# Kernel tuning notes

Hardware: AMD Instinct MI355X
Metric: run time of the kernel (lower is better)

## Reference

```python
import jax, jax.numpy as jnp
from jax import lax
import numpy as np

B, N, G, K = 4, 1024, 128, 32
D_MODEL, DEPTH, CLS = 384, 12, 40
D_INNER, D_STATE, D_CONV, DT_RANK = 768, 16, 4, 24
EPS = 1e-5
BN_SCALE = 1.0 / float(np.sqrt(1.0 + EPS))  # eval BN, running_mean=0, running_var=1


def layernorm(x, w, b):
    mu = x.mean(-1, keepdims=True)
    var = ((x - mu) ** 2).mean(-1, keepdims=True)
    return (x - mu) * lax.rsqrt(var + EPS) * w + b


def bn_eval(x, g, b):
    return x * (g * BN_SCALE) + b


def fps(xyz, n):
    Bb, Nn, _ = xyz.shape
    first = jnp.zeros((Bb,), jnp.int32)

    def step(carry, _):
        dmin, last = carry
        p = jnp.take_along_axis(xyz, last[:, None, None], axis=1)  # B,1,3
        dmin = jnp.minimum(dmin, jnp.sum((xyz - p) ** 2, -1))
        nxt = jnp.argmax(dmin, -1).astype(jnp.int32)
        return (dmin, nxt), nxt

    _, rest = lax.scan(step, (jnp.full((Bb, Nn), 1e10, xyz.dtype), first), None, length=n - 1)
    return jnp.concatenate([first[None, :], rest], 0).T  # B,G


def group_points(xyz):
    idx = fps(xyz, G)
    center = jnp.take_along_axis(xyz, idx[:, :, None], axis=1)            # B,G,3
    d2 = jnp.sum((center[:, :, None, :] - xyz[:, None, :, :]) ** 2, -1)   # B,G,N
    _, knn = lax.top_k(-d2, K)                                            # B,G,K
    nb = jax.vmap(lambda p, i: p[i])(xyz, knn)                            # B,G,K,3
    return nb - center[:, :, None, :], center


def encoder(pg, w1, b1, g1, bb1, w2, b2, w3, b3, g2, bb2, w4, b4):
    Bb, Gg, Kk, _ = pg.shape
    f = pg.reshape(Bb * Gg, Kk, 3)
    f = jax.nn.relu(bn_eval(f @ w1.T + b1, g1, bb1))                      # BG,K,128
    f = f @ w2.T + b2                                                     # BG,K,256
    fg = f.max(1, keepdims=True)
    f = jnp.concatenate([jnp.broadcast_to(fg, f.shape), f], -1)           # BG,K,512
    f = jax.nn.relu(bn_eval(f @ w3.T + b3, g2, bb2))
    f = f @ w4.T + b4
    return f.max(1).reshape(Bb, Gg, -1)                                   # B,G,C


def mamba_mixer(x, ipw, cw, cb, xpw, dpw, dpb, A_log, Dp, opw):
    L = x.shape[1]
    xz = x @ ipw.T                                                        # B,L,2*Di
    u, z = jnp.split(xz, 2, -1)
    up = jnp.pad(u, ((0, 0), (D_CONV - 1, 0), (0, 0)))                    # causal depthwise conv
    u = sum(up[:, k:k + L, :] * cw[:, k] for k in range(D_CONV)) + cb
    u = jax.nn.silu(u)
    xdb = u @ xpw.T
    dt, Bm, Cm = jnp.split(xdb, [DT_RANK, DT_RANK + D_STATE], -1)
    dt = jax.nn.softplus(dt @ dpw.T + dpb)                                # B,L,Di
    A = -jnp.exp(A_log)                                                   # Di,Ds

    def step(h, inp):
        dt_t, B_t, C_t, u_t = inp
        h = jnp.exp(dt_t[:, :, None] * A) * h + (dt_t * u_t)[:, :, None] * B_t[:, None, :]
        return h, jnp.einsum('bds,bs->bd', h, C_t)

    h0 = jnp.zeros((x.shape[0], D_INNER, D_STATE), x.dtype)
    _, ys = lax.scan(step, h0, (dt.swapaxes(0, 1), Bm.swapaxes(0, 1), Cm.swapaxes(0, 1), u.swapaxes(0, 1)))
    y = ys.swapaxes(0, 1) + u * Dp
    return (y * jax.nn.silu(z)) @ opw.T


def forward(pts, enc_w1, enc_b1, enc_bn1_g, enc_bn1_b, enc_w2, enc_b2, enc_w3, enc_b3,
            enc_bn2_g, enc_bn2_b, enc_w4, enc_b4, pos_w1, pos_b1, pos_w2, pos_b2,
            ln_w, ln_b, in_proj_w, conv_w, conv_b, x_proj_w, dt_proj_w, dt_proj_b,
            A_log, D_param, out_proj_w, normf_w, normf_b, norm_w, norm_b,
            head_w1, head_b1, head_bn1_g, head_bn1_b, head_w2, head_b2,
            head_bn2_g, head_bn2_b, head_w3, head_b3):
    nb, center = group_points(pts)
    tok = encoder(nb, enc_w1, enc_b1, enc_bn1_g, enc_bn1_b, enc_w2, enc_b2,
                  enc_w3, enc_b3, enc_bn2_g, enc_bn2_b, enc_w4, enc_b4)    # B,G,384
    pos = jax.nn.gelu(center @ pos_w1.T + pos_b1, approximate=False) @ pos_w2.T + pos_b2

    # PointMamba token reordering: sort by center x, y, z and concatenate -> L = 3G
    toks, poss = [], []
    for ax in range(3):
        o = jnp.argsort(center[:, :, ax], axis=-1)[:, :, None]
        toks.append(jnp.take_along_axis(tok, o, axis=1))
        poss.append(jnp.take_along_axis(pos, o, axis=1))
    tok = jnp.concatenate(toks, 1)
    pos = jnp.concatenate(poss, 1)

    h = tok + pos
    res = jnp.zeros_like(h)

    def layer_step(carry, p):
        h, res = carry
        lnw, lnb, ipw, cw, cb, xpw, dpw, dpb, Al, Dp, opw = p
        res = h + res
        x = layernorm(res, lnw, lnb)
        h = mamba_mixer(x, ipw, cw, cb, xpw, dpw, dpb, Al, Dp, opw)
        return (h, res), None

    (h, res), _ = lax.scan(layer_step, (h, res),
                           (ln_w, ln_b, in_proj_w, conv_w, conv_b, x_proj_w,
                            dt_proj_w, dt_proj_b, A_log, D_param, out_proj_w))
    x = layernorm(h + res, normf_w, normf_b)   # MixerModel.norm_f
    x = layernorm(x, norm_w, norm_b)           # PointMamba.norm
    feat = x.mean(1)                           # B,384
    h1 = jax.nn.relu(bn_eval(feat @ head_w1.T + head_b1, head_bn1_g, head_bn1_b))
    h2 = jax.nn.relu(bn_eval(h1 @ head_w2.T + head_b2, head_bn2_g, head_bn2_b))
    return h2 @ head_w3.T + head_b3            # B,CLS


def setup_inputs():
    key = jax.random.key(0)
    ks = iter(jax.random.split(key, 64))

    def rn(shape, s=0.02):
        return jax.random.normal(next(ks), shape, jnp.float32) * s

    inp = dict(
        pts=jax.random.normal(next(ks), (B, N, 3), jnp.float32),
        enc_w1=rn((128, 3), 0.1), enc_b1=jnp.zeros((128,)),
        enc_bn1_g=jnp.ones((128,)), enc_bn1_b=jnp.zeros((128,)),
        enc_w2=rn((256, 128), 0.05), enc_b2=jnp.zeros((256,)),
        enc_w3=rn((512, 512), 0.05), enc_b3=jnp.zeros((512,)),
        enc_bn2_g=jnp.ones((512,)), enc_bn2_b=jnp.zeros((512,)),
        enc_w4=rn((D_MODEL, 512), 0.05), enc_b4=jnp.zeros((D_MODEL,)),
        pos_w1=rn((128, 3), 0.1), pos_b1=jnp.zeros((128,)),
        pos_w2=rn((D_MODEL, 128), 0.05), pos_b2=jnp.zeros((D_MODEL,)),
        ln_w=jnp.ones((DEPTH, D_MODEL)), ln_b=jnp.zeros((DEPTH, D_MODEL)),
        in_proj_w=rn((DEPTH, 2 * D_INNER, D_MODEL)),
        conv_w=rn((DEPTH, D_INNER, D_CONV), 0.2), conv_b=jnp.zeros((DEPTH, D_INNER)),
        x_proj_w=rn((DEPTH, DT_RANK + 2 * D_STATE, D_INNER)),
        dt_proj_w=rn((DEPTH, D_INNER, DT_RANK), 0.1),
        dt_proj_b=jnp.full((DEPTH, D_INNER), -4.6, jnp.float32),
        A_log=jnp.broadcast_to(jnp.log(jnp.arange(1, D_STATE + 1, dtype=jnp.float32)),
                               (DEPTH, D_INNER, D_STATE)).copy(),
        D_param=jnp.ones((DEPTH, D_INNER)),
        out_proj_w=rn((DEPTH, D_MODEL, D_INNER)),
        normf_w=jnp.ones((D_MODEL,)), normf_b=jnp.zeros((D_MODEL,)),
        norm_w=jnp.ones((D_MODEL,)), norm_b=jnp.zeros((D_MODEL,)),
        head_w1=rn((256, D_MODEL), 0.05), head_b1=jnp.zeros((256,)),
        head_bn1_g=jnp.ones((256,)), head_bn1_b=jnp.zeros((256,)),
        head_w2=rn((256, 256), 0.05), head_b2=jnp.zeros((256,)),
        head_bn2_g=jnp.ones((256,)), head_bn2_b=jnp.zeros((256,)),
        head_w3=rn((CLS, 256), 0.05), head_b3=jnp.zeros((CLS,)),
    )
    return inp


def reference(pts, enc_w1, enc_b1, enc_bn1_g, enc_bn1_b, enc_w2, enc_b2, enc_w3, enc_b3,
              enc_bn2_g, enc_bn2_b, enc_w4, enc_b4, pos_w1, pos_b1, pos_w2, pos_b2,
              ln_w, ln_b, in_proj_w, conv_w, conv_b, x_proj_w, dt_proj_w, dt_proj_b,
              A_log, D_param, out_proj_w, normf_w, normf_b, norm_w, norm_b,
              head_w1, head_b1, head_bn1_g, head_bn1_b, head_w2, head_b2,
              head_bn2_g, head_bn2_b, head_w3, head_b3):
    return forward(pts, enc_w1, enc_b1, enc_bn1_g, enc_bn1_b, enc_w2, enc_b2, enc_w3, enc_b3,
                   enc_bn2_g, enc_bn2_b, enc_w4, enc_b4, pos_w1, pos_b1, pos_w2, pos_b2,
                   ln_w, ln_b, in_proj_w, conv_w, conv_b, x_proj_w, dt_proj_w, dt_proj_b,
                   A_log, D_param, out_proj_w, normf_w, normf_b, norm_w, norm_b,
                   head_w1, head_b1, head_bn1_g, head_bn1_b, head_w2, head_b2,
                   head_bn2_g, head_bn2_b, head_w3, head_b3)
```

## Files before the change

kernel.cpp:

```cpp
#include <hip/hip_runtime.h>
#include <hip/hip_bf16.h>

using bf16 = __hip_bfloat16;
using short8  = __attribute__((ext_vector_type(8))) short;
using floatx4 = __attribute__((ext_vector_type(4))) float;
using ull = unsigned long long;

constexpr int Bn = 4, Np = 1024, Gn = 128, Kn = 32;
constexpr int DM = 384, DEPTH = 12, CLSn = 40;
constexpr int DI = 768, DSt = 16, DTR = 24;
constexpr int Ln = 384;
constexpr int NCH = 12, CHS = 32;
constexpr int XDBS = 1536*56;
constexpr float EPSf = 1e-5f;
constexpr float BNS = 0.99999500003749968752f;
constexpr float LOG2E = 1.4426950408889634f;

static __device__ __forceinline__ short f2bf(float f){
  bf16 h = __float2bfloat16(f);
  return *reinterpret_cast<short*>(&h);
}
static __device__ __forceinline__ float fsig(float x){ return 1.f/(1.f + __expf(-x)); }
static __device__ __forceinline__ float fsoftplus(float x){
  return fmaxf(x, 0.f) + __logf(1.f + __expf(-fabsf(x)));
}
static __device__ __forceinline__ ull umax64(ull a, ull b){ return a > b ? a : b; }

template<int CTRL>
static __device__ __forceinline__ int dppmov(int x){
  return __builtin_amdgcn_update_dpp(0, x, CTRL, 0xF, 0xF, true);
}
static __device__ __forceinline__ ull redmax64(ull key){
  #define RSTEP(CTRL) { \
    int hi = (int)(unsigned)(key >> 32), lo = (int)(unsigned)key; \
    int h2 = dppmov<CTRL>(hi), l2 = dppmov<CTRL>(lo); \
    ull k2 = ((ull)(unsigned)h2 << 32) | (unsigned)l2; \
    if (k2 > key) key = k2; }
  RSTEP(0x111) RSTEP(0x112) RSTEP(0x114) RSTEP(0x118) RSTEP(0x142) RSTEP(0x143)
  #undef RSTEP
  return key;
}

__global__ __launch_bounds__(256) void fps_kernel(const float* __restrict__ pts,
                                                  float* __restrict__ center){
  int b = blockIdx.x, t = threadIdx.x;
  int w = t >> 6, lane = t & 63;
  __shared__ float4 P[1024];
  __shared__ ull red[2][4];
  const float* p = pts + (size_t)b * Np * 3;
  float X[4], Y[4], Z[4], D[4];
  #pragma unroll
  for (int i = 0; i < 4; ++i){
    int n = t + 256*i;
    float a = p[n*3+0], c = p[n*3+1], e = p[n*3+2];
    X[i] = a; Y[i] = c; Z[i] = e;
    P[n] = make_float4(a, c, e, 0.f);
    D[i] = 1e10f;
  }
  __syncthreads();
  float4 c0 = P[0];
  float px = c0.x, py = c0.y, pz = c0.z;
  if (t == 0){
    center[(size_t)(b*Gn)*3+0] = px;
    center[(size_t)(b*Gn)*3+1] = py;
    center[(size_t)(b*Gn)*3+2] = pz;
  }
  for (int it = 1; it < Gn; ++it){
    float v = -1.f; int nbest = t;
    #pragma unroll
    for (int i = 0; i < 4; ++i){
      float dx = __fsub_rn(X[i], px);
      float dy = __fsub_rn(Y[i], py);
      float dz = __fsub_rn(Z[i], pz);
      float d  = __fadd_rn(__fadd_rn(__fmul_rn(dx,dx), __fmul_rn(dy,dy)), __fmul_rn(dz,dz));
      float dm = fminf(D[i], d); D[i] = dm;
      if (dm > v){ v = dm; nbest = t + 256*i; }
    }
    ull key = ((ull)__float_as_uint(v) << 32) | (unsigned)(Np-1 - nbest);
    key = redmax64(key);
    if (lane == 63) red[it & 1][w] = key;
    __syncthreads();
    ull k = umax64(umax64(red[it & 1][0], red[it & 1][1]),
                   umax64(red[it & 1][2], red[it & 1][3]));
    int wn = Np-1 - (int)(unsigned)(k & 0xFFFFFFFFu);
    wn = min(max(wn, 0), Np-1);
    float4 cc = P[wn];
    px = cc.x; py = cc.y; pz = cc.z;
    if (t == 0){
      center[(size_t)(b*Gn+it)*3+0] = px;
      center[(size_t)(b*Gn+it)*3+1] = py;
      center[(size_t)(b*Gn+it)*3+2] = pz;
    }
  }
}

__global__ __launch_bounds__(256) void knn_kernel(const float* __restrict__ pts,
                                                  const float* __restrict__ center,
                                                  float* __restrict__ nb){
  int gid = blockIdx.x; int b = gid >> 7;
  __shared__ float d2[1024];
  __shared__ float rv[4]; __shared__ int ri[4];
  int t = threadIdx.x;
  float cx = center[(size_t)gid*3+0], cy = center[(size_t)gid*3+1], cz = center[(size_t)gid*3+2];
  const float* p = pts + (size_t)b * Np * 3;
  for (int n = t; n < Np; n += 256){
    float dx = __fsub_rn(cx, p[n*3+0]);
    float dy = __fsub_rn(cy, p[n*3+1]);
    float dz = __fsub_rn(cz, p[n*3+2]);
    d2[n] = __fadd_rn(__fadd_rn(__fmul_rn(dx,dx), __fmul_rn(dy,dy)), __fmul_rn(dz,dz));
  }
  __syncthreads();
  for (int kk = 0; kk < Kn; ++kk){
    float v = 3e38f; int idx = 0;
    for (int n = t; n < Np; n += 256){
      float d = d2[n];
      if (d < v || (d == v && n < idx)){ v = d; idx = n; }
    }
    ull key = ((ull)(unsigned)(~__float_as_uint(v)) << 32) | (unsigned)(Np-1 - idx);
    key = redmax64(key);
    if ((t & 63) == 63){
      rv[t>>6] = __uint_as_float(~(unsigned)(key >> 32));
      ri[t>>6] = Np-1 - (int)(unsigned)(key & 0xFFFFFFFFu);
    }
    __syncthreads();
    if (t == 0){
      float bv = rv[0]; int bi = ri[0];
      for (int w = 1; w < 4; ++w){
        if (rv[w] < bv || (rv[w] == bv && ri[w] < bi)){ bv = rv[w]; bi = ri[w]; }
      }
      bi = min(max(bi, 0), Np-1);
      nb[((size_t)gid*Kn+kk)*3+0] = __fsub_rn(p[bi*3+0], cx);
      nb[((size_t)gid*Kn+kk)*3+1] = __fsub_rn(p[bi*3+1], cy);
      nb[((size_t)gid*Kn+kk)*3+2] = __fsub_rn(p[bi*3+2], cz);
      d2[bi] = 3e38f;
    }
    __syncthreads();
  }
}

__global__ __launch_bounds__(256) void cvt_all(const float* __restrict__ s0,
    const float* __restrict__ s1, const float* __restrict__ s2,
    const float* __restrict__ s3, const float* __restrict__ s4,
    const float* __restrict__ s5, bf16* __restrict__ dst){
  long i = ((long)blockIdx.x*256 + threadIdx.x)*4;
  if (i >= 11624448L) return;
  const float* s; long off;
  if      (i <  7077888L){ s = s0; off = 0L; }
  else if (i < 10616832L){ s = s1; off =  7077888L; }
  else if (i < 11132928L){ s = s2; off = 10616832L; }
  else if (i < 11165696L){ s = s3; off = 11132928L; }
  else if (i < 11427840L){ s = s4; off = 11165696L; }
  else                   { s = s5; off = 11427840L; }
  float4 v = *(const float4*)(s + (i - off));
  short* o = (short*)dst + i;
  o[0] = f2bf(v.x); o[1] = f2bf(v.y); o[2] = f2bf(v.z); o[3] = f2bf(v.w);
}

template<typename AT, typename WT, int ACT, int MODE, typename CT = float>
__global__ __launch_bounds__(256) void gemm_mfma(const AT* __restrict__ A, int lda,
                                                 const WT* __restrict__ W,
                                                 const float* __restrict__ bias,
                                                 const float* __restrict__ gz,
                                                 const float* __restrict__ bbp,
                                                 CT* __restrict__ C, int ldc,
                                                 int M, int N, int K){
  __shared__ __align__(16) short As[64*40];
  __shared__ __align__(16) short Ws[64*40];
  int bm = blockIdx.x * 64, bn = blockIdx.y * 64;
  int t = threadIdx.x;
  int row = t >> 2;
  int kseg = (t & 3) * 8;
  int w = t >> 6, lane = t & 63, m16 = lane & 15, q = lane >> 4;
  floatx4 acc[4] = {};
  for (int k0 = 0; k0 < K; k0 += 32){
    {
      const float* Ar = (const float*)A + (size_t)(bm + row)*lda;
      short* dst = &As[row*40 + kseg];
      #pragma unroll
      for (int j = 0; j < 8; ++j){
        int k = k0 + kseg + j;
        dst[j] = (k < K) ? f2bf(Ar[k]) : (short)0;
      }
    }
    {
      int n = bn + row;
      short* dst = &Ws[row*40 + kseg];
      #pragma unroll
      for (int j = 0; j < 8; ++j){
        int k = k0 + kseg + j;
        dst[j] = (n < N && k < K) ? f2bf(((const float*)W)[(size_t)n*K + k]) : (short)0;
      }
    }
    __syncthreads();
    short8 af = *(const short8*)&As[(w*16 + m16)*40 + q*8];
    #pragma unroll
    for (int j = 0; j < 4; ++j){
      short8 bfr = *(const short8*)&Ws[(j*16 + m16)*40 + q*8];
      acc[j] = __builtin_amdgcn_mfma_f32_16x16x32_bf16(af, bfr, acc[j], 0, 0, 0);
    }
    __syncthreads();
  }
  #pragma unroll
  for (int j = 0; j < 4; ++j){
    int n = bn + j*16 + m16;
    if (n < N){
      float bv = bias ? bias[n] : 0.f;
      float gv = 0.f, bbv = 0.f;
      if (ACT == 1){ gv = gz[n] * BNS; bbv = bbp[n]; }
      #pragma unroll
      for (int r = 0; r < 4; ++r){
        int m = bm + w*16 + q*4 + r;
        float v = acc[j][r] + bv;
        if (ACT == 1){ v = v * gv + bbv; v = fmaxf(v, 0.f); }
        if constexpr (sizeof(CT) == 2) C[(size_t)m*ldc + n] = __float2bfloat16(v);
        else                           C[(size_t)m*ldc + n] = v;
      }
    }
  }
}

template<typename AT, typename WT, int ACT, int MODE, typename CT = float>
__global__ __launch_bounds__(256) void gemm_mfma64(const AT* __restrict__ A, int lda,
                                                   const WT* __restrict__ W,
                                                   const float* __restrict__ bias,
                                                   const float* __restrict__ gz,
                                                   const float* __restrict__ bbp,
                                                   CT* __restrict__ C, int ldc,
                                                   int M, int N, int K){
  __shared__ __align__(16) short As[64*72];
  __shared__ __align__(16) short Ws[64*72];
  int bm = blockIdx.x * 64, bn = blockIdx.y * 64;
  int t = threadIdx.x;
  int row = t >> 2;
  int kseg = (t & 3) * 16;
  int w = t >> 6, lane = t & 63, m16 = lane & 15, q = lane >> 4;
  floatx4 acc[4] = {};
  for (int k0 = 0; k0 < K; k0 += 64){
    if constexpr (MODE == 1){
      const float* Yr = (const float*)A + (size_t)(bm + row)*lda + k0 + kseg;
      const float* Zr = gz + (size_t)(bm + row)*1536 + 768 + k0 + kseg;
      float y[16], z[16];
      #pragma unroll
      for (int j = 0; j < 4; ++j){
        *(float4*)&y[j*4] = *(const float4*)(Yr + j*4);
        *(float4*)&z[j*4] = *(const float4*)(Zr + j*4);
      }
      short* dst = &As[row*72 + kseg];
      #pragma unroll
      for (int jj = 0; jj < 16; ++jj) dst[jj] = f2bf(y[jj] * (z[jj] * fsig(z[jj])));
    } else if constexpr (sizeof(AT) == 2){
      const short* Ar = (const short*)A + (size_t)(bm + row)*lda + k0 + kseg;
      *(short8*)&As[row*72 + kseg]     = *(const short8*)Ar;
      *(short8*)&As[row*72 + kseg + 8] = *(const short8*)(Ar + 8);
    } else {
      const float* Ar = (const float*)A + (size_t)(bm + row)*lda + k0 + kseg;
      float a[16];
      #pragma unroll
      for (int j = 0; j < 4; ++j) *(float4*)&a[j*4] = *(const float4*)(Ar + j*4);
      short* dst = &As[row*72 + kseg];
      #pragma unroll
      for (int jj = 0; jj < 16; ++jj) dst[jj] = f2bf(a[jj]);
    }
    {
      int n = bn + row;
      if constexpr (sizeof(WT) == 2){
        short8 v0, v1;
        #pragma unroll
        for (int j = 0; j < 8; ++j){ v0[j] = 0; v1[j] = 0; }
        if (n < N){
          const short* Wr = (const short*)W + (size_t)n*K + k0 + kseg;
          v0 = *(const short8*)Wr;
          v1 = *(const short8*)(Wr + 8);
        }
        *(short8*)&Ws[row*72 + kseg]     = v0;
        *(short8*)&Ws[row*72 + kseg + 8] = v1;
      } else {
        short* dst = &Ws[row*72 + kseg];
        if (n < N){
          const float* Wr = (const float*)W + (size_t)n*K + k0 + kseg;
          float wv[16];
          #pragma unroll
          for (int j = 0; j < 4; ++j) *(float4*)&wv[j*4] = *(const float4*)(Wr + j*4);
          #pragma unroll
          for (int jj = 0; jj < 16; ++jj) dst[jj] = f2bf(wv[jj]);
        } else {
          #pragma unroll
          for (int jj = 0; jj < 16; ++jj) dst[jj] = 0;
        }
      }
    }
    __syncthreads();
    short8 af0 = *(const short8*)&As[(w*16 + m16)*72 + q*8];
    short8 af1 = *(const short8*)&As[(w*16 + m16)*72 + 32 + q*8];
    #pragma unroll
    for (int j = 0; j < 4; ++j){
      short8 b0 = *(const short8*)&Ws[(j*16 + m16)*72 + q*8];
      acc[j] = __builtin_amdgcn_mfma_f32_16x16x32_bf16(af0, b0, acc[j], 0, 0, 0);
      short8 b1 = *(const short8*)&Ws[(j*16 + m16)*72 + 32 + q*8];
      acc[j] = __builtin_amdgcn_mfma_f32_16x16x32_bf16(af1, b1, acc[j], 0, 0, 0);
    }
    __syncthreads();
  }
  #pragma unroll
  for (int j = 0; j < 4; ++j){
    int n = bn + j*16 + m16;
    if (n < N){
      float bv = bias ? bias[n] : 0.f;
      float gv = 0.f, bbv = 0.f;
      if (ACT == 1){ gv = gz[n] * BNS; bbv = bbp[n]; }
      #pragma unroll
      for (int r = 0; r < 4; ++r){
        int m = bm + w*16 + q*4 + r;
        float v = acc[j][r] + bv;
        if (ACT == 1){ v = v * gv + bbv; v = fmaxf(v, 0.f); }
        if constexpr (sizeof(CT) == 2) C[(size_t)m*ldc + n] = __float2bfloat16(v);
        else                           C[(size_t)m*ldc + n] = v;
      }
    }
  }
}

template<typename AT, typename WT, int ACT, typename CT, int POOL>
__global__ __launch_bounds__(256) void gemm_mfma128(const AT* __restrict__ A, int lda,
                                                    const WT* __restrict__ W,
                                                    const float* __restrict__ bias,
                                                    const float* __restrict__ gz,
                                                    const float* __restrict__ bbp,
                                                    CT* __restrict__ C, int ldc,
                                                    int M, int N, int K){
  __shared__ __align__(16) short As[64*72];
  __shared__ __align__(16) short Ws[128*72];
  int bm = blockIdx.x * 64, bn = blockIdx.y * 128;
  int t = threadIdx.x;
  int row = t >> 2;
  int kseg = (t & 3) * 16;
  int row2 = t >> 1;
  int kseg2 = (t & 1) * 32;
  int w = t >> 6, lane = t & 63, m16 = lane & 15, q = lane >> 4;
  floatx4 acc[8] = {};
  for (int k0 = 0; k0 < K; k0 += 64){
    if constexpr (sizeof(AT) == 2){
      const short* Ar = (const short*)A + (size_t)(bm + row)*lda + k0 + kseg;
      *(short8*)&As[row*72 + kseg]     = *(const short8*)Ar;
      *(short8*)&As[row*72 + kseg + 8] = *(const short8*)(Ar + 8);
    } else {
      const float* Ar = (const float*)A + (size_t)(bm + row)*lda + k0 + kseg;
      float a[16];
      #pragma unroll
      for (int j = 0; j < 4; ++j) *(float4*)&a[j*4] = *(const float4*)(Ar + j*4);
      short* dst = &As[row*72 + kseg];
      #pragma unroll
      for (int jj = 0; jj < 16; ++jj) dst[jj] = f2bf(a[jj]);
    }
    {
      int n = bn + row2;
      if constexpr (sizeof(WT) == 2){
        short8 v0, v1, v2, v3;
        #pragma unroll
        for (int j = 0; j < 8; ++j){ v0[j] = 0; v1[j] = 0; v2[j] = 0; v3[j] = 0; }
        if (n < N){
          const short* Wr = (const short*)W + (size_t)n*K + k0 + kseg2;
          v0 = *(const short8*)Wr;
          v1 = *(const short8*)(Wr + 8);
          v2 = *(const short8*)(Wr + 16);
          v3 = *(const short8*)(Wr + 24);
        }
        *(short8*)&Ws[row2*72 + kseg2]      = v0;
        *(short8*)&Ws[row2*72 + kseg2 + 8]  = v1;
        *(short8*)&Ws[row2*72 + kseg2 + 16] = v2;
        *(short8*)&Ws[row2*72 + kseg2 + 24] = v3;
      } else {
        short* dst = &Ws[row2*72 + kseg2];
        if (n < N){
          const float* Wr = (const float*)W + (size_t)n*K + k0 + kseg2;
          float wv[32];
          #pragma unroll
          for (int j = 0; j < 8; ++j) *(float4*)&wv[j*4] = *(const float4*)(Wr + j*4);
          #pragma unroll
          for (int jj = 0; jj < 32; ++jj) dst[jj] = f2bf(wv[jj]);
        } else {
          #pragma unroll
          for (int jj = 0; jj < 32; ++jj) dst[jj] = 0;
        }
      }
    }
    __syncthreads();
    short8 af0 = *(const short8*)&As[(w*16 + m16)*72 + q*8];
    short8 af1 = *(const short8*)&As[(w*16 + m16)*72 + 32 + q*8];
    #pragma unroll
    for (int j = 0; j < 8; ++j){
      short8 b0 = *(const short8*)&Ws[(j*16 + m16)*72 + q*8];
      acc[j] = __builtin_amdgcn_mfma_f32_16x16x32_bf16(af0, b0, acc[j], 0, 0, 0);
      short8 b1 = *(const short8*)&Ws[(j*16 + m16)*72 + 32 + q*8];
      acc[j] = __builtin_amdgcn_mfma_f32_16x16x32_bf16(af1, b1, acc[j], 0, 0, 0);
    }
    __syncthreads();
  }
  float val[8][4];
  #pragma unroll
  for (int j = 0; j < 8; ++j){
    int n = bn + j*16 + m16;
    float bv = (bias && n < N) ? bias[n] : 0.f;
    float gv = 0.f, bbv = 0.f;
    if (ACT == 1 && n < N){ gv = gz[n] * BNS; bbv = bbp[n]; }
    #pragma unroll
    for (int r = 0; r < 4; ++r){
      float v = acc[j][r] + bv;
      if (ACT == 1){ v = v * gv + bbv; v = fmaxf(v, 0.f); }
      val[j][r] = v;
    }
  }
  if constexpr (POOL == 0){
    #pragma unroll
    for (int j = 0; j < 8; ++j){
      int n = bn + j*16 + m16;
      if (n < N){
        #pragma unroll
        for (int r = 0; r < 4; ++r){
          int m = bm + w*16 + q*4 + r;
          if constexpr (sizeof(CT) == 2) C[(size_t)m*ldc + n] = __float2bfloat16(val[j][r]);
          else                           C[(size_t)m*ldc + n] = val[j][r];
        }
      }
    }
  } else {
    float* mat = (float*)As;
    #pragma unroll
    for (int j = 0; j < 8; ++j){
      float lm = fmaxf(fmaxf(val[j][0], val[j][1]), fmaxf(val[j][2], val[j][3]));
      mat[(w*4 + q)*128 + j*16 + m16] = lm;
    }
    if constexpr (POOL == 1){
      #pragma unroll
      for (int j = 0; j < 8; ++j){
        int n = bn + j*16 + m16;
        #pragma unroll
        for (int r = 0; r < 4; ++r){
          int m = bm + w*16 + q*4 + r;
          C[(size_t)m*ldc + n] = __float2bfloat16(val[j][r]);
        }
      }
    }
    __syncthreads();
    int col = t & 127, half = t >> 7;
    float gm = mat[(half*8)*128 + col];
    #pragma unroll
    for (int s = 1; s < 8; ++s) gm = fmaxf(gm, mat[(half*8 + s)*128 + col]);
    if constexpr (POOL == 1){
      bf16 gb = __float2bfloat16(gm);
      bf16* dst = (bf16*)C - 256 + (size_t)(bm + half*32)*ldc + bn + col;
      #pragma unroll
      for (int rr = 0; rr < 32; ++rr) dst[(size_t)rr*ldc] = gb;
    } else {
      int g = (bm >> 5) + half;
      ((float*)C)[(size_t)g*ldc + bn + col] = gm;
    }
  }
}

template<typename WT>
__global__ __launch_bounds__(256) void xproj_kernel(const float* __restrict__ xz,
                                                    const WT* __restrict__ W,
                                                    const float* __restrict__ cw,
                                                    const float* __restrict__ cb,
                                                    float* __restrict__ xdbp,
                                                    int KB){
  __shared__ __align__(16) short As[64*72];
  __shared__ __align__(16) short Ws[64*72];
  int bm = blockIdx.x * 64;
  int ks = blockIdx.y;
  int t = threadIdx.x;
  int row = t >> 2, kseg = (t & 3) * 16;
  int w = t >> 6, lane = t & 63, m16 = lane & 15, q = lane >> 4;
  int m = bm + row;
  int l = m % Ln;
  const int kbase = ks * KB;
  floatx4 acc[4] = {};
  const float4 z4 = make_float4(0.f, 0.f, 0.f, 0.f);
  for (int k0 = kbase; k0 < kbase + KB; k0 += 64){
    {
      int ch = k0 + kseg;
      const float* base = xz + (size_t)m*1536 + ch;
      float x0[16], x1[16], x2[16], x3[16];
      #pragma unroll
      for (int j4 = 0; j4 < 4; ++j4){
        *(float4*)&x3[j4*4] = *(const float4*)(base + j4*4);
        *(float4*)&x2[j4*4] = (l >= 1) ? *(const float4*)(base - 1536 + j4*4) : z4;
        *(float4*)&x1[j4*4] = (l >= 2) ? *(const float4*)(base - 2*1536 + j4*4) : z4;
        *(float4*)&x0[j4*4] = (l >= 3) ? *(const float4*)(base - 3*1536 + j4*4) : z4;
      }
      short* dst = &As[row*72 + kseg];
      #pragma unroll
      for (int j = 0; j < 16; ++j){
        float4 wv = *(const float4*)(cw + (size_t)(ch + j)*4);
        float v = x0[j]*wv.x + x1[j]*wv.y + x2[j]*wv.z + x3[j]*wv.w + cb[ch + j];
        v = v * fsig(v);
        dst[j] = f2bf(v);
      }
    }
    {
      int n = row;
      if constexpr (sizeof(WT) == 2){
        short8 v0, v1;
        #pragma unroll
        for (int j = 0; j < 8; ++j){ v0[j] = 0; v1[j] = 0; }
        if (n < 56){
          const short* Wr = (const short*)W + (size_t)n*DI + k0 + kseg;
          v0 = *(const short8*)Wr;
          v1 = *(const short8*)(Wr + 8);
        }
        *(short8*)&Ws[row*72 + kseg]     = v0;
        *(short8*)&Ws[row*72 + kseg + 8] = v1;
      } else {
        short* dst = &Ws[row*72 + kseg];
        if (n < 56){
          const float* Wr = (const float*)W + (size_t)n*DI + k0 + kseg;
          float wv[16];
          #pragma unroll
          for (int j = 0; j < 4; ++j) *(float4*)&wv[j*4] = *(const float4*)(Wr + j*4);
          #pragma unroll
          for (int jj = 0; jj < 16; ++jj) dst[jj] = f2bf(wv[jj]);
        } else {
          #pragma unroll
          for (int jj = 0; jj < 16; ++jj) dst[jj] = 0;
        }
      }
    }
    __syncthreads();
    short8 af0 = *(const short8*)&As[(w*16 + m16)*72 + q*8];
    short8 af1 = *(const short8*)&As[(w*16 + m16)*72 + 32 + q*8];
    #pragma unroll
    for (int j = 0; j < 4; ++j){
      short8 b0 = *(const short8*)&Ws[(j*16 + m16)*72 + q*8];
      acc[j] = __builtin_amdgcn_mfma_f32_16x16x32_bf16(af0, b0, acc[j], 0, 0, 0);
      short8 b1 = *(const short8*)&Ws[(j*16 + m16)*72 + 32 + q*8];
      acc[j] = __builtin_amdgcn_mfma_f32_16x16x32_bf16(af1, b1, acc[j], 0, 0, 0);
    }
    __syncthreads();
  }
  float* C = xdbp + (size_t)ks * XDBS;
  #pragma unroll
  for (int j = 0; j < 4; ++j){
    int n = j*16 + m16;
    if (n < 56){
      #pragma unroll
      for (int r = 0; r < 4; ++r){
        int mm = bm + w*16 + q*4 + r;
        C[(size_t)mm*56 + n] = acc[j][r];
      }
    }
  }
}

__global__ __launch_bounds__(256) void maxk_fg(float* __restrict__ f3in){
  int gg = blockIdx.x; int c = threadIdx.x;
  float m = -3e38f;
  for (int k = 0; k < Kn; ++k) m = fmaxf(m, f3in[((size_t)gg*Kn + k)*512 + 256 + c]);
  for (int k = 0; k < Kn; ++k) f3in[((size_t)gg*Kn + k)*512 + c] = m;
}

__global__ __launch_bounds__(384) void maxk_tok(const float* __restrict__ f4, float* __restrict__ tok){
  int gg = blockIdx.x; int c = threadIdx.x;
  float m = -3e38f;
  for (int k = 0; k < Kn; ++k) m = fmaxf(m, f4[((size_t)gg*Kn + k)*DM + c]);
  tok[(size_t)gg*DM + c] = m;
}

__global__ __launch_bounds__(128) void pos_kernel(const float* __restrict__ center,
                                                  const float* __restrict__ w1, const float* __restrict__ b1,
                                                  const float* __restrict__ w2, const float* __restrict__ b2,
                                                  float* __restrict__ tok){
  int gid = blockIdx.x;
  __shared__ float h1[128]; __shared__ float c3[3];
  int t = threadIdx.x;
  if (t < 3) c3[t] = center[(size_t)gid*3 + t];
  __syncthreads();
  float a = w1[t*3+0]*c3[0] + w1[t*3+1]*c3[1] + w1[t*3+2]*c3[2] + b1[t];
  h1[t] = 0.5f * a * (1.f + erff(a * 0.70710678118654752440f));
  __syncthreads();
  for (int c = t; c < DM; c += 128){
    float s = b2[c];
    for (int j = 0; j < 128; ++j) s += w2[(size_t)c*128 + j] * h1[j];
    tok[(size_t)gid*DM + c] += s;
  }
}

__global__ __launch_bounds__(128) void sort_kernel(const float* __restrict__ center,
                                                   int* __restrict__ order){
  int bax = blockIdx.x; int b = bax / 3, ax = bax % 3;
  __shared__ float key[128];
  int t = threadIdx.x;
  key[t] = center[(size_t)(b*Gn + t)*3 + ax];
  __syncthreads();
  float kt = key[t]; int r = 0;
  for (int j = 0; j < Gn; ++j){
    float kj = key[j];
    r += (kj < kt || (kj == kt && j < t)) ? 1 : 0;
  }
  r = min(max(r, 0), Gn-1);
  order[b*Ln + ax*Gn + r] = t;
}

__global__ __launch_bounds__(256) void build_h(const float* __restrict__ tok,
                        const int* __restrict__ order,
                        float* __restrict__ h, float* __restrict__ res){
  int i = blockIdx.x * blockDim.x + threadIdx.x;
  if (i >= Bn*Ln*DM) return;
  int c = i % DM; int l = (i / DM) % Ln; int b = i / (DM*Ln);
  int src = order[b*Ln + l];
  src = min(max(src, 0), Gn-1);
  h[i] = tok[((size_t)(b*Gn + src))*DM + c];
  res[i] = 0.f;
}

__global__ __launch_bounds__(256) void ln_res_kernel(const float* __restrict__ h,
                                                     float* __restrict__ res,
                                                     bf16* __restrict__ x,
                                                     const float* __restrict__ w,
                                                     const float* __restrict__ bias){
  int wv = threadIdx.x >> 6, ln = threadIdx.x & 63;
  int tokid = blockIdx.x*4 + wv;
  const float* hr = h + (size_t)tokid*DM;
  float* rr = res + (size_t)tokid*DM;
  bf16* xr = x + (size_t)tokid*DM;
  float v[6]; float s = 0.f;
  #pragma unroll
  for (int i = 0; i < 6; ++i){ int c = ln + 64*i; float t = hr[c] + rr[c]; rr[c] = t; v[i] = t; s += t; }
  #pragma unroll
  for (int o = 32; o > 0; o >>= 1) s += __shfl_xor(s, o);
  float mu = s * (1.f/DM);
  float q = 0.f;
  #pragma unroll
  for (int i = 0; i < 6; ++i){ float d = v[i] - mu; q += d*d; }
  #pragma unroll
  for (int o = 32; o > 0; o >>= 1) q += __shfl_xor(q, o);
  float rstd = rsqrtf(q * (1.f/DM) + EPSf);
  #pragma unroll
  for (int i = 0; i < 6; ++i){ int c = ln + 64*i;
    xr[c] = __float2bfloat16((v[i]-mu)*rstd*w[c] + bias[c]); }
}

__global__ __launch_bounds__(256) void scanA_kernel(const float* __restrict__ xz,
                                                    const float* __restrict__ xdbp, int nks,
                                                    const float* __restrict__ cw,
                                                    const float* __restrict__ cb,
                                                    const float* __restrict__ dpw,
                                                    const float* __restrict__ dpb,
                                                    const float* __restrict__ A_log,
                                                    float* __restrict__ SB_S,
                                                    float* __restrict__ SB_dt,
                                                    float* __restrict__ BND){
  __shared__ float sRow[CHS*56];
  __shared__ float sU[CHS*256];
  int blk = blockIdx.x;
  int c = blk % NCH; int bd = blk / NCH; int dch = bd % 3; int b = bd / 3;
  int t = threadIdx.x; int d = dch*256 + t;
  int l0 = c*CHS;
  for (int i = t; i < CHS*56; i += 256){
    size_t base = ((size_t)(b*Ln + l0))*56 + i;
    float s = xdbp[base];
    for (int k = 1; k < nks; ++k) s += xdbp[(size_t)k*XDBS + base];
    sRow[i] = s;
  }
  float xv[CHS+3];
  #pragma unroll
  for (int j = 0; j < 3; ++j){
    int ll = l0 - 3 + j;
    xv[j] = (ll >= 0) ? xz[((size_t)(b*Ln + ll))*1536 + d] : 0.f;
  }
  const float* xp = xz + ((size_t)(b*Ln + l0))*1536 + d;
  #pragma unroll
  for (int i = 0; i < CHS; ++i) xv[3+i] = xp[(size_t)i*1536];
  #pragma unroll
  for (int j = 0; j < 3; ++j) BND[((size_t)blk*3 + j)*256 + t] = xv[j];
  float cw0 = cw[d*4+0], cw1 = cw[d*4+1], cw2 = cw[d*4+2], cw3 = cw[d*4+3];
  float cbv = cb[d];
  #pragma unroll
  for (int i = 0; i < CHS; ++i){
    float v = xv[i]*cw0 + xv[i+1]*cw1 + xv[i+2]*cw2 + xv[i+3]*cw3 + cbv;
    sU[i*256 + t] = v * fsig(v);
  }
  float w[DTR];
  const float* wp = dpw + (size_t)d*DTR;
  #pragma unroll
  for (int j = 0; j < DTR; ++j) w[j] = wp[j];
  float a2[DSt], h[DSt];
  const float* ap = A_log + (size_t)d*DSt;
  #pragma unroll
  for (int s = 0; s < DSt; ++s){ a2[s] = -__expf(ap[s]) * LOG2E; h[s] = 0.f; }
  float dbias = dpb[d];
  float sumdt = 0.f;
  __syncthreads();
  for (int i = 0; i < CHS; ++i){
    int ro = i*56;
    float dtr = dbias;
    #pragma unroll
    for (int j = 0; j < DTR; ++j) dtr += w[j] * sRow[ro + j];
    float dtv = fsoftplus(dtr);
    sumdt += dtv;
    float du = dtv * sU[i*256 + t];
    #pragma unroll
    for (int s = 0; s < DSt; ++s)
      h[s] = exp2f(dtv * a2[s]) * h[s] + du * sRow[ro + 24 + s];
  }
  size_t sb = ((size_t)blk*256 + t)*16;
  #pragma unroll
  for (int s = 0; s < DSt; ++s) SB_S[sb + s] = h[s];
  SB_dt[(size_t)blk*256 + t] = sumdt;
}

__global__ __launch_bounds__(256) void scanB_kernel(float* __restrict__ xz,
                                                    const float* __restrict__ xdbp, int nks,
                                                    const float* __restrict__ cw,
                                                    const float* __restrict__ cb,
                                                    const float* __restrict__ dpw,
                                                    const float* __restrict__ dpb,
                                                    const float* __restrict__ A_log,
                                                    const float* __restrict__ Dp,
                                                    const float* __restrict__ SB_S,
                                                    const float* __restrict__ SB_dt,
                                                    const float* __restrict__ BND,
                                                    bf16* __restrict__ yb){
  __shared__ float sRow[CHS*56];
  __shared__ float sU[CHS*256];
  int blk = blockIdx.x;
  int c = blk % NCH; int bd = blk / NCH; int dch = bd % 3; int b = bd / 3;
  int t = threadIdx.x; int d = dch*256 + t;
  int l0 = c*CHS;
  for (int i = t; i < CHS*56; i += 256){
    size_t base = ((size_t)(b*Ln + l0))*56 + i;
    float s = xdbp[base];
    for (int k = 1; k < nks; ++k) s += xdbp[(size_t)k*XDBS + base];
    sRow[i] = s;
  }
  float xv[CHS+3];
  #pragma unroll
  for (int j = 0; j < 3; ++j) xv[j] = BND[((size_t)blk*3 + j)*256 + t];
  const float* xp = xz + ((size_t)(b*Ln + l0))*1536 + d;
  #pragma unroll
  for (int i = 0; i < CHS; ++i) xv[3+i] = xp[(size_t)i*1536];
  float cw0 = cw[d*4+0], cw1 = cw[d*4+1], cw2 = cw[d*4+2], cw3 = cw[d*4+3];
  float cbv = cb[d];
  #pragma unroll
  for (int i = 0; i < CHS; ++i){
    float v = xv[i]*cw0 + xv[i+1]*cw1 + xv[i+2]*cw2 + xv[i+3]*cw3 + cbv;
    sU[i*256 + t] = v * fsig(v);
  }
  float w[DTR];
  const float* wp = dpw + (size_t)d*DTR;
  #pragma unroll
  for (int j = 0; j < DTR; ++j) w[j] = wp[j];
  float a2[DSt], h[DSt];
  const float* ap = A_log + (size_t)d*DSt;
  #pragma unroll
  for (int s = 0; s < DSt; ++s){ a2[s] = -__expf(ap[s]) * LOG2E; h[s] = 0.f; }
  for (int cc = 0; cc < c; ++cc){
    size_t base = (((size_t)bd*NCH + cc)*256 + t)*16;
    float sd = SB_dt[((size_t)bd*NCH + cc)*256 + t];
    #pragma unroll
    for (int s = 0; s < DSt; ++s)
      h[s] = exp2f(sd * a2[s]) * h[s] + SB_S[base + s];
  }
  float dbias = dpb[d];
  float Dd = Dp[d];
  float* ydst = xz + ((size_t)(b*Ln + l0))*1536 + dch*256;
  const float* zrow = xz + ((size_t)(b*Ln + l0))*1536 + 768 + dch*256;
  bf16* ybr = yb ? (yb + ((size_t)(b*Ln + l0))*DI + dch*256) : nullptr;
  __syncthreads();
  for (int i = 0; i < CHS; ++i){
    int ro = i*56;
    float dtr = dbias;
    #pragma unroll
    for (int j = 0; j < DTR; ++j) dtr += w[j] * sRow[ro + j];
    float dtv = fsoftplus(dtr);
    float u = sU[i*256 + t];
    float du = dtv * u;
    float yv = 0.f;
    #pragma unroll
    for (int s = 0; s < DSt; ++s){
      h[s] = exp2f(dtv * a2[s]) * h[s] + du * sRow[ro + 24 + s];
      yv += h[s] * sRow[ro + 40 + s];
    }
    float yfull = yv + u*Dd;
    if (ybr){
      float zv = zrow[(size_t)i*1536 + t];
      ybr[(size_t)i*DI + t] = __float2bfloat16(yfull * (zv * fsig(zv)));
    } else {
      ydst[(size_t)i*1536 + t] = yfull;
    }
  }
}

__global__ __launch_bounds__(256) void final_ln_kernel(const float* __restrict__ h,
                                                       const float* __restrict__ res,
                                                       const float* w1, const float* b1,
                                                       const float* w2, const float* b2,
                                                       float* __restrict__ x){
  int wv = threadIdx.x >> 6, ln = threadIdx.x & 63;
  int tokid = blockIdx.x*4 + wv;
  const float* hr = h + (size_t)tokid*DM;
  const float* rr = res + (size_t)tokid*DM;
  float* xr = x + (size_t)tokid*DM;
  float v[6]; float s = 0.f;
  #pragma unroll
  for (int i = 0; i < 6; ++i){ int c = ln + 64*i; v[i] = hr[c] + rr[c]; s += v[i]; }
  #pragma unroll
  for (int o = 32; o > 0; o >>= 1) s += __shfl_xor(s, o);
  float mu = s * (1.f/DM); float q = 0.f;
  #pragma unroll
  for (int i = 0; i < 6; ++i){ float dd = v[i]-mu; q += dd*dd; }
  #pragma unroll
  for (int o = 32; o > 0; o >>= 1) q += __shfl_xor(q, o);
  float rstd = rsqrtf(q * (1.f/DM) + EPSf);
  float u[6]; float s2 = 0.f;
  #pragma unroll
  for (int i = 0; i < 6; ++i){ int c = ln + 64*i; u[i] = (v[i]-mu)*rstd*w1[c] + b1[c]; s2 += u[i]; }
  #pragma unroll
  for (int o = 32; o > 0; o >>= 1) s2 += __shfl_xor(s2, o);
  float mu2 = s2 * (1.f/DM); float q2 = 0.f;
  #pragma unroll
  for (int i = 0; i < 6; ++i){ float dd = u[i]-mu2; q2 += dd*dd; }
  #pragma unroll
  for (int o = 32; o > 0; o >>= 1) q2 += __shfl_xor(q2, o);
  float rstd2 = rsqrtf(q2 * (1.f/DM) + EPSf);
  #pragma unroll
  for (int i = 0; i < 6; ++i){ int c = ln + 64*i; xr[c] = (u[i]-mu2)*rstd2*w2[c] + b2[c]; }
}

__global__ __launch_bounds__(384) void mean_kernel(const float* __restrict__ x,
                                                   float* __restrict__ featp){
  int blk = blockIdx.x;
  int b = blk >> 2, g = blk & 3;
  int c = threadIdx.x;
  const float* xp = x + ((size_t)(b*Ln + g*96))*DM + c;
  float a0=0.f,a1=0.f,a2=0.f,a3=0.f,a4=0.f,a5=0.f,a6=0.f,a7=0.f;
  for (int l = 0; l < 96; l += 8){
    a0 += xp[(size_t)(l+0)*DM];
    a1 += xp[(size_t)(l+1)*DM];
    a2 += xp[(size_t)(l+2)*DM];
    a3 += xp[(size_t)(l+3)*DM];
    a4 += xp[(size_t)(l+4)*DM];
    a5 += xp[(size_t)(l+5)*DM];
    a6 += xp[(size_t)(l+6)*DM];
    a7 += xp[(size_t)(l+7)*DM];
  }
  featp[(size_t)blk*DM + c] = ((a0+a1)+(a2+a3)) + ((a4+a5)+(a6+a7));
}

__global__ __launch_bounds__(256) void head_mlp(const float* __restrict__ featp,
    const float* w1, const float* b1, const float* g1, const float* bb1,
    const float* w2, const float* b2, const float* g2, const float* bb2,
    const float* w3, const float* b3, float* __restrict__ out){
  int b = blockIdx.x; int t = threadIdx.x;
  __shared__ float f[DM]; __shared__ float h1[256]; __shared__ float h2[256];
  for (int i = t; i < DM; i += 256){
    f[i] = (featp[(size_t)(b*4+0)*DM + i] + featp[(size_t)(b*4+1)*DM + i]
          + featp[(size_t)(b*4+2)*DM + i] + featp[(size_t)(b*4+3)*DM + i]) * (1.f/Ln);
  }
  __syncthreads();
  {
    float a = b1[t];
    #pragma unroll 4
    for (int j = 0; j < DM; ++j) a += w1[(size_t)t*DM + j] * f[j];
    a = a * (g1[t] * BNS) + bb1[t];
    h1[t] = fmaxf(a, 0.f);
  }
  __syncthreads();
  {
    float a = b2[t];
    #pragma unroll 4
    for (int j = 0; j < 256; ++j) a += w2[(size_t)t*256 + j] * h1[j];
    a = a * (g2[t] * BNS) + bb2[t];
    h2[t] = fmaxf(a, 0.f);
  }
  __syncthreads();
  if (t < CLSn){
    float a = b3[t];
    for (int j = 0; j < 256; ++j) a += w3[(size_t)t*256 + j] * h2[j];
    out[b*CLSn + t] = a;
  }
}

extern "C" void kernel_launch(void* const* d_in, const int* in_sizes, int n_in,
                              void* d_out, int out_size, void* d_ws, size_t ws_size,
                              hipStream_t stream) {
  if (n_in < 42) return;
  if (out_size < Bn*CLSn) return;
  constexpr size_t WS_FLOATS = 3919936;
  if (ws_size < WS_FLOATS * sizeof(float)) return;
  constexpr size_t MIDF = 5812224;
  constexpr size_t BIGF = 9437184;
  const bool mid = ws_size >= (WS_FLOATS + MIDF) * sizeof(float);
  const bool big = ws_size >= (WS_FLOATS + MIDF + BIGF) * sizeof(float);

  const float* pts       = (const float*)d_in[0];
  const float* enc_w1    = (const float*)d_in[1];  const float* enc_b1    = (const float*)d_in[2];
  const float* enc_bn1_g = (const float*)d_in[3];  const float* enc_bn1_b = (const float*)d_in[4];
  const float* enc_w2    = (const float*)d_in[5];  const float* enc_b2    = (const float*)d_in[6];
  const float* enc_w3    = (const float*)d_in[7];  const float* enc_b3    = (const float*)d_in[8];
  const float* enc_bn2_g = (const float*)d_in[9];  const float* enc_bn2_b = (const float*)d_in[10];
  const float* enc_w4    = (const float*)d_in[11]; const float* enc_b4    = (const float*)d_in[12];
  const float* pos_w1    = (const float*)d_in[13]; const float* pos_b1    = (const float*)d_in[14];
  const float* pos_w2    = (const float*)d_in[15]; const float* pos_b2    = (const float*)d_in[16];
  const float* ln_w      = (const float*)d_in[17]; const float* ln_b      = (const float*)d_in[18];
  const float* in_proj_w = (const float*)d_in[19];
  const float* conv_w    = (const float*)d_in[20]; const float* conv_b    = (const float*)d_in[21];
  const float* x_proj_w  = (const float*)d_in[22];
  const float* dt_proj_w = (const float*)d_in[23]; const float* dt_proj_b = (const float*)d_in[24];
  const float* A_log     = (const float*)d_in[25]; const float* D_param   = (const float*)d_in[26];
  const float* out_proj_w= (const float*)d_in[27];
  const float* normf_w   = (const float*)d_in[28]; const float* normf_b   = (const float*)d_in[29];
  const float* norm_w    = (const float*)d_in[30]; const float* norm_b    = (const float*)d_in[31];
  const float* head_w1   = (const float*)d_in[32]; const float* head_b1   = (const float*)d_in[33];
  const float* head_bn1_g= (const float*)d_in[34]; const float* head_bn1_b= (const float*)d_in[35];
  const float* head_w2   = (const float*)d_in[36]; const float* head_b2   = (const float*)d_in[37];
  const float* head_bn2_g= (const float*)d_in[38]; const float* head_bn2_b= (const float*)d_in[39];
  const float* head_w3   = (const float*)d_in[40]; const float* head_b3   = (const float*)d_in[41];

  float* ws = (float*)d_ws;
  float* hb   = ws;
  float* resb = ws + 589824;
  float* U    = ws + 1179648;
  float* center = U;
  float* nb     = U + 1536;
  float* tok    = U + 50688;
  int*   order  = (int*)(U + 247296);
  float* eb0    = U + 262144;
  float* eb1    = U + 1310720;
  float* xz   = U;
  float* xdb  = U + 2359296;
  bf16*  xb   = (bf16*)(U + 2445312);
  float* SBdt_s = U + 2445312;
  float* BND  = U + 2482176;
  float* SBS_s  = hb;
  float* xf   = U;
  float* featp = U + 589824;
  float* WB = ws + WS_FLOATS;
  bf16* wb_ip = (bf16*)WB;
  bf16* wb_op = (bf16*)(WB + 3538944);
  bf16* wb_xp = (bf16*)(WB + 5308416);
  bf16* wb_e2 = (bf16*)(WB + 5566464);
  bf16* wb_e3 = (bf16*)(WB + 5582848);
  bf16* wb_e4 = (bf16*)(WB + 5713920);
  float* BIGB = WB + MIDF;
  bf16*  F1b  = (bf16*)BIGB;
  bf16*  F3b  = (bf16*)(BIGB + 1048576);
  bf16*  F3c  = (bf16*)(BIGB + 5242880);
  float* xdbp_b = BIGB;
  float* SBS_b  = BIGB + 344064;
  float* SBdt_b = BIGB + 933888;
  bf16*  yb     = (bf16*)(BIGB + 970752);

  if (mid)
    cvt_all<<<11352, 256, 0, stream>>>(in_proj_w, out_proj_w, x_proj_w,
                                       enc_w2, enc_w3, enc_w4, (bf16*)WB);

  fps_kernel<<<Bn, 256, 0, stream>>>(pts, center);
  knn_kernel<<<Bn*Gn, 256, 0, stream>>>(pts, center, nb);

  if (big){
    gemm_mfma<float,float,1,0,bf16><<<dim3(256,2), 256, 0, stream>>>(nb, 3, enc_w1, enc_b1,
        enc_bn1_g, enc_bn1_b, F1b, 128, 16384, 128, 3);
    gemm_mfma128<bf16,bf16,0,bf16,1><<<dim3(256,2), 256, 0, stream>>>(F1b, 128, wb_e2, enc_b2,
        nullptr, nullptr, F3b + 256, 512, 16384, 256, 128);
    gemm_mfma128<bf16,bf16,1,bf16,0><<<dim3(256,4), 256, 0, stream>>>(F3b, 512, wb_e3, enc_b3,
        enc_bn2_g, enc_bn2_b, F3c, 512, 16384, 512, 512);
    gemm_mfma128<bf16,bf16,0,float,2><<<dim3(256,3), 256, 0, stream>>>(F3c, 512, wb_e4, enc_b4,
        nullptr, nullptr, tok, DM, 16384, 384, 512);
  } else {
    for (int ch = 0; ch < 8; ++ch){
      const float* nb_c = nb + (size_t)ch*2048*3;
      float* tok_c = tok + (size_t)ch*64*DM;
      gemm_mfma<float,float,1,0><<<dim3(32,2), 256, 0, stream>>>(nb_c, 3, enc_w1, enc_b1,
          enc_bn1_g, enc_bn1_b, eb1, 128, 2048, 128, 3);
      if (mid){
        gemm_mfma64<float,bf16,0,0><<<dim3(32,4), 256, 0, stream>>>(eb1, 128, wb_e2, enc_b2,
            nullptr, nullptr, eb0 + 256, 512, 2048, 256, 128);
        maxk_fg<<<64, 256, 0, stream>>>(eb0);
        gemm_mfma64<float,bf16,1,0><<<dim3(32,8), 256, 0, stream>>>(eb0, 512, wb_e3, enc_b3,
            enc_bn2_g, enc_bn2_b, eb1, 512, 2048, 512, 512);
        gemm_mfma64<float,bf16,0,0><<<dim3(32,6), 256, 0, stream>>>(eb1, 512, wb_e4, enc_b4,
            nullptr, nullptr, eb0, 384, 2048, 384, 512);
      } else {
        gemm_mfma64<float,float,0,0><<<dim3(32,4), 256, 0, stream>>>(eb1, 128, enc_w2, enc_b2,
            nullptr, nullptr, eb0 + 256, 512, 2048, 256, 128);
        maxk_fg<<<64, 256, 0, stream>>>(eb0);
        gemm_mfma64<float,float,1,0><<<dim3(32,8), 256, 0, stream>>>(eb0, 512, enc_w3, enc_b3,
            enc_bn2_g, enc_bn2_b, eb1, 512, 2048, 512, 512);
        gemm_mfma64<float,float,0,0><<<dim3(32,6), 256, 0, stream>>>(eb1, 512, enc_w4, enc_b4,
            nullptr, nullptr, eb0, 384, 2048, 384, 512);
      }
      maxk_tok<<<64, 384, 0, stream>>>(eb0, tok_c);
    }
  }

  pos_kernel<<<Bn*Gn, 128, 0, stream>>>(center, pos_w1, pos_b1, pos_w2, pos_b2, tok);
  sort_kernel<<<Bn*3, 128, 0, stream>>>(center, order);
  build_h<<<(Bn*Ln*DM + 255)/256, 256, 0, stream>>>(tok, order, hb, resb);

  const int nks = big ? 4 : 1;
  float* xdbp = big ? xdbp_b : xdb;
  float* SBS  = big ? SBS_b  : SBS_s;
  float* SBdt = big ? SBdt_b : SBdt_s;

  for (int l = 0; l < DEPTH; ++l){
    const float* lnw  = ln_w      + (size_t)l*DM;
    const float* lnb  = ln_b      + (size_t)l*DM;
    const float* ipw  = in_proj_w + (size_t)l*1536*DM;
    const float* cw   = conv_w    + (size_t)l*DI*4;
    const float* cb   = conv_b    + (size_t)l*DI;
    const float* xpw  = x_proj_w  + (size_t)l*56*DI;
    const float* dpw  = dt_proj_w + (size_t)l*DI*DTR;
    const float* dpb  = dt_proj_b + (size_t)l*DI;
    const float* Alg  = A_log     + (size_t)l*DI*DSt;
    const float* Dpar = D_param   + (size_t)l*DI;
    const float* opw  = out_proj_w+ (size_t)l*DM*DI;

    ln_res_kernel<<<Bn*Ln/4, 256, 0, stream>>>(hb, resb, xb, lnw, lnb);
    if (mid){
      gemm_mfma128<bf16,bf16,0,float,0><<<dim3(24,12), 256, 0, stream>>>(xb, DM,
          wb_ip + (size_t)l*1536*DM, nullptr, nullptr, nullptr, xz, 1536, Bn*Ln, 1536, DM);
    } else {
      gemm_mfma128<bf16,float,0,float,0><<<dim3(24,12), 256, 0, stream>>>(xb, DM, ipw,
          nullptr, nullptr, nullptr, xz, 1536, Bn*Ln, 1536, DM);
    }
    if (mid)
      xproj_kernel<bf16><<<dim3(24, nks), 256, 0, stream>>>(xz,
          wb_xp + (size_t)l*56*DI, cw, cb, xdbp, DI/nks);
    else
      xproj_kernel<float><<<dim3(24, nks), 256, 0, stream>>>(xz,
          xpw, cw, cb, xdbp, DI/nks);
    scanA_kernel<<<Bn*3*NCH, 256, 0, stream>>>(xz, xdbp, nks, cw, cb,
        dpw, dpb, Alg, SBS, SBdt, BND);
    scanB_kernel<<<Bn*3*NCH, 256, 0, stream>>>(xz, xdbp, nks, cw, cb,
        dpw, dpb, Alg, Dpar, SBS, SBdt, BND, big ? yb : nullptr);
    if (big){
      gemm_mfma64<bf16,bf16,0,0><<<dim3(24,6), 256, 0, stream>>>(yb, DI,
          wb_op + (size_t)l*DM*DI, nullptr, nullptr, nullptr, hb, DM, Bn*Ln, DM, DI);
    } else if (mid){
      gemm_mfma64<float,bf16,0,1><<<dim3(24,6), 256, 0, stream>>>(xz, 1536,
          wb_op + (size_t)l*DM*DI, nullptr, xz, nullptr, hb, DM, Bn*Ln, DM, DI);
    } else {
      gemm_mfma64<float,float,0,1><<<dim3(24,6), 256, 0, stream>>>(xz, 1536, opw,
          nullptr, xz, nullptr, hb, DM, Bn*Ln, DM, DI);
    }
  }

  final_ln_kernel<<<Bn*Ln/4, 256, 0, stream>>>(hb, resb, normf_w, normf_b, norm_w, norm_b, xf);
  mean_kernel<<<Bn*4, 384, 0, stream>>>(xf, featp);
  head_mlp<<<Bn, 256, 0, stream>>>(featp, head_w1, head_b1, head_bn1_g, head_bn1_b,
                                   head_w2, head_b2, head_bn2_g, head_bn2_b,
                                   head_w3, head_b3, (float*)d_out);
}
```

Before: 1.801 ms.

## Fuse front-end kernels and restructure encoder into per-batch chunks

Merges the weight bf16 conversion into the FPS launch, and fuses the first encoder layer (3->128 with BN/ReLU) into the second GEMM together with the K-max broadcast. The encoder now runs in four per-batch chunks of 4096 rows using the 128-wide GEMM with bf16 intermediates. It merges the pos and sort kernels and folds build_h into a first-layer LayerNorm kernel. It also drops the large-workspace path with split-K x_proj and the fused bf16 gated output, which cuts launch count and intermediate traffic but may cost in the Mamba layers wherever the big path used to be selected.

```diff
diff --git a/kernel.cpp b/kernel.cpp
--- a/kernel.cpp
+++ b/kernel.cpp
@@ -12,6 +12,7 @@
 constexpr int Ln = 384;
 constexpr int NCH = 12, CHS = 32;
 constexpr int XDBS = 1536*56;
+constexpr int MC = 4096;
 constexpr float EPSf = 1e-5f;
 constexpr float BNS = 0.99999500003749968752f;
 constexpr float LOG2E = 1.4426950408889634f;
@@ -41,12 +42,31 @@
   return key;
 }
 
-__global__ __launch_bounds__(256) void fps_kernel(const float* __restrict__ pts,
-                                                  float* __restrict__ center){
+__global__ __launch_bounds__(256) void front_kernel(const float* __restrict__ pts,
+    float* __restrict__ center,
+    const float* __restrict__ s0, const float* __restrict__ s1,
+    const float* __restrict__ s2, const float* __restrict__ s3,
+    const float* __restrict__ s4, const float* __restrict__ s5,
+    bf16* __restrict__ dst){
+  __shared__ float4 P[1024];
+  __shared__ ull red[2][4];
+  if (blockIdx.x >= Bn){
+    long i = ((long)(blockIdx.x - Bn)*256 + threadIdx.x)*4;
+    if (i >= 11624448L) return;
+    const float* s; long off;
+    if      (i <  7077888L){ s = s0; off = 0L; }
+    else if (i < 10616832L){ s = s1; off =  7077888L; }
+    else if (i < 11132928L){ s = s2; off = 10616832L; }
+    else if (i < 11165696L){ s = s3; off = 11132928L; }
+    else if (i < 11427840L){ s = s4; off = 11165696L; }
+    else                   { s = s5; off = 11427840L; }
+    float4 v = *(const float4*)(s + (i - off));
+    short* o = (short*)dst + i;
+    o[0] = f2bf(v.x); o[1] = f2bf(v.y); o[2] = f2bf(v.z); o[3] = f2bf(v.w);
+    return;
+  }
   int b = blockIdx.x, t = threadIdx.x;
   int w = t >> 6, lane = t & 63;
-  __shared__ float4 P[1024];
-  __shared__ ull red[2][4];
   const float* p = pts + (size_t)b * Np * 3;
   float X[4], Y[4], Z[4], D[4];
   #pragma unroll
@@ -138,186 +158,103 @@
   }
 }
 
-__global__ __launch_bounds__(256) void cvt_all(const float* __restrict__ s0,
-    const float* __restrict__ s1, const float* __restrict__ s2,
-    const float* __restrict__ s3, const float* __restrict__ s4,
-    const float* __restrict__ s5, bf16* __restrict__ dst){
-  long i = ((long)blockIdx.x*256 + threadIdx.x)*4;
-  if (i >= 11624448L) return;
-  const float* s; long off;
-  if      (i <  7077888L){ s = s0; off = 0L; }
-  else if (i < 10616832L){ s = s1; off =  7077888L; }
-  else if (i < 11132928L){ s = s2; off = 10616832L; }
-  else if (i < 11165696L){ s = s3; off = 11132928L; }
-  else if (i < 11427840L){ s = s4; off = 11165696L; }
-  else                   { s = s5; off = 11427840L; }
-  float4 v = *(const float4*)(s + (i - off));
-  short* o = (short*)dst + i;
-  o[0] = f2bf(v.x); o[1] = f2bf(v.y); o[2] = f2bf(v.z); o[3] = f2bf(v.w);
-}
-
-template<typename AT, typename WT, int ACT, int MODE, typename CT = float>
-__global__ __launch_bounds__(256) void gemm_mfma(const AT* __restrict__ A, int lda,
-                                                 const WT* __restrict__ W,
-                                                 const float* __restrict__ bias,
-                                                 const float* __restrict__ gz,
-                                                 const float* __restrict__ bbp,
-                                                 CT* __restrict__ C, int ldc,
-                                                 int M, int N, int K){
-  __shared__ __align__(16) short As[64*40];
-  __shared__ __align__(16) short Ws[64*40];
-  int bm = blockIdx.x * 64, bn = blockIdx.y * 64;
+template<typename WT>
+__global__ __launch_bounds__(256) void enc2_kernel(const float* __restrict__ nb,
+    const float* __restrict__ w1, const float* __restrict__ b1,
+    const float* __restrict__ g1, const float* __restrict__ bb1,
+    const WT* __restrict__ W2, const float* __restrict__ b2,
+    bf16* __restrict__ F3b){
+  __shared__ __align__(16) short As[64*72];
+  __shared__ __align__(16) short Ws[128*72];
+  __shared__ float w1s0[128], w1s1[128], w1s2[128], sa[128], sc[128];
+  int bm = blockIdx.x * 64, bn = blockIdx.y * 128;
   int t = threadIdx.x;
-  int row = t >> 2;
-  int kseg = (t & 3) * 8;
+  int row = t >> 2, kseg = (t & 3) * 16;
+  int row2 = t >> 1, kseg2 = (t & 1) * 32;
   int w = t >> 6, lane = t & 63, m16 = lane & 15, q = lane >> 4;
-  floatx4 acc[4] = {};
-  for (int k0 = 0; k0 < K; k0 += 32){
+  if (t < 128){
+    float a = g1[t] * BNS;
+    w1s0[t] = w1[t*3+0]; w1s1[t] = w1[t*3+1]; w1s2[t] = w1[t*3+2];
+    sa[t] = a; sc[t] = b1[t]*a + bb1[t];
+  }
+  const float* nbr = nb + (size_t)(bm + row)*3;
+  float p0 = nbr[0], p1 = nbr[1], p2 = nbr[2];
+  __syncthreads();
+  floatx4 acc[8] = {};
+  for (int k0 = 0; k0 < 128; k0 += 64){
     {
-      const float* Ar = (const float*)A + (size_t)(bm + row)*lda;
-      short* dst = &As[row*40 + kseg];
+      short* dstp = &As[row*72 + kseg];
       #pragma unroll
-      for (int j = 0; j < 8; ++j){
-        int k = k0 + kseg + j;
-        dst[j] = (k < K) ? f2bf(Ar[k]) : (short)0;
+      for (int j = 0; j < 16; ++j){
+        int c = k0 + kseg + j;
+        float v = p0*w1s0[c] + p1*w1s1[c] + p2*w1s2[c];
+        v = fmaxf(v*sa[c] + sc[c], 0.f);
+        dstp[j] = f2bf(v);
       }
     }
     {
-      int n = bn + row;
-      short* dst = &Ws[row*40 + kseg];
-      #pragma unroll
-      for (int j = 0; j < 8; ++j){
-        int k = k0 + kseg + j;
-        dst[j] = (n < N && k < K) ? f2bf(((const float*)W)[(size_t)n*K + k]) : (short)0;
-      }
-    }
-    __syncthreads();
-    short8 af = *(const short8*)&As[(w*16 + m16)*40 + q*8];
-    #pragma unroll
-    for (int j = 0; j < 4; ++j){
-      short8 bfr = *(const short8*)&Ws[(j*16 + m16)*40 + q*8];
-      acc[j] = __builtin_amdgcn_mfma_f32_16x16x32_bf16(af, bfr, acc[j], 0, 0, 0);
-    }
-    __syncthreads();
-  }
-  #pragma unroll
-  for (int j = 0; j < 4; ++j){
-    int n = bn + j*16 + m16;
-    if (n < N){
-      float bv = bias ? bias[n] : 0.f;
-      float gv = 0.f, bbv = 0.f;
-      if (ACT == 1){ gv = gz[n] * BNS; bbv = bbp[n]; }
-      #pragma unroll
-      for (int r = 0; r < 4; ++r){
-        int m = bm + w*16 + q*4 + r;
-        float v = acc[j][r] + bv;
-        if (ACT == 1){ v = v * gv + bbv; v = fmaxf(v, 0.f); }
-        if constexpr (sizeof(CT) == 2) C[(size_t)m*ldc + n] = __float2bfloat16(v);
-        else                           C[(size_t)m*ldc + n] = v;
-      }
-    }
-  }
-}
-
-template<typename AT, typename WT, int ACT, int MODE, typename CT = float>
-__global__ __launch_bounds__(256) void gemm_mfma64(const AT* __restrict__ A, int lda,
-                                                   const WT* __restrict__ W,
-                                                   const float* __restrict__ bias,
-                                                   const float* __restrict__ gz,
-                                                   const float* __restrict__ bbp,
-                                                   CT* __restrict__ C, int ldc,
-                                                   int M, int N, int K){
-  __shared__ __align__(16) short As[64*72];
-  __shared__ __align__(16) short Ws[64*72];
-  int bm = blockIdx.x * 64, bn = blockIdx.y * 64;
-  int t = threadIdx.x;
-  int row = t >> 2;
-  int kseg = (t & 3) * 16;
-  int w = t >> 6, lane = t & 63, m16 = lane & 15, q = lane >> 4;
-  floatx4 acc[4] = {};
-  for (int k0 = 0; k0 < K; k0 += 64){
-    if constexpr (MODE == 1){
-      const float* Yr = (const float*)A + (size_t)(bm + row)*lda + k0 + kseg;
-      const float* Zr = gz + (size_t)(bm + row)*1536 + 768 + k0 + kseg;
-      float y[16], z[16];
-      #pragma unroll
-      for (int j = 0; j < 4; ++j){
-        *(float4*)&y[j*4] = *(const float4*)(Yr + j*4);
-        *(float4*)&z[j*4] = *(const float4*)(Zr + j*4);
-      }
-      short* dst = &As[row*72 + kseg];
-      #pragma unroll
-      for (int jj = 0; jj < 16; ++jj) dst[jj] = f2bf(y[jj] * (z[jj] * fsig(z[jj])));
-    } else if constexpr (sizeof(AT) == 2){
-      const short* Ar = (const short*)A + (size_t)(bm + row)*lda + k0 + kseg;
-      *(short8*)&As[row*72 + kseg]     = *(const short8*)Ar;
-      *(short8*)&As[row*72 + kseg + 8] = *(const short8*)(Ar + 8);
-    } else {
-      const float* Ar = (const float*)A + (size_t)(bm + row)*lda + k0 + kseg;
-      float a[16];
-      #pragma unroll
-      for (int j = 0; j < 4; ++j) *(float4*)&a[j*4] = *(const float4*)(Ar + j*4);
-      short* dst = &As[row*72 + kseg];
-      #pragma unroll
-      for (int jj = 0; jj < 16; ++jj) dst[jj] = f2bf(a[jj]);
-    }
-    {
-      int n = bn + row;
+      int n = bn + row2;
       if constexpr (sizeof(WT) == 2){
-        short8 v0, v1;
+        const short* Wr = (const short*)W2 + (size_t)n*128 + k0 + kseg2;
+        *(short8*)&Ws[row2*72 + kseg2]      = *(const short8*)Wr;
+        *(short8*)&Ws[row2*72 + kseg2 + 8]  = *(const short8*)(Wr + 8);
+        *(short8*)&Ws[row2*72 + kseg2 + 16] = *(const short8*)(Wr + 16);
+        *(short8*)&Ws[row2*72 + kseg2 + 24] = *(const short8*)(Wr + 24);
+      } else {
+        const float* Wr = (const float*)W2 + (size_t)n*128 + k0 + kseg2;
+        float wv[32];
         #pragma unroll
-        for (int j = 0; j < 8; ++j){ v0[j] = 0; v1[j] = 0; }
-        if (n < N){
-          const short* Wr = (const short*)W + (size_t)n*K + k0 + kseg;
-          v0 = *(const short8*)Wr;
-          v1 = *(const short8*)(Wr + 8);
-        }
-        *(short8*)&Ws[row*72 + kseg]     = v0;
-        *(short8*)&Ws[row*72 + kseg + 8] = v1;
-      } else {
-        short* dst = &Ws[row*72 + kseg];
-        if (n < N){
-          const float* Wr = (const float*)W + (size_t)n*K + k0 + kseg;
-          float wv[16];
-          #pragma unroll
-          for (int j = 0; j < 4; ++j) *(float4*)&wv[j*4] = *(const float4*)(Wr + j*4);
-          #pragma unroll
-          for (int jj = 0; jj < 16; ++jj) dst[jj] = f2bf(wv[jj]);
-        } else {
-          #pragma unroll
-          for (int jj = 0; jj < 16; ++jj) dst[jj] = 0;
-        }
+        for (int j = 0; j < 8; ++j) *(float4*)&wv[j*4] = *(const float4*)(Wr + j*4);
+        short* dstp = &Ws[row2*72 + kseg2];
+        #pragma unroll
+        for (int jj = 0; jj < 32; ++jj) dstp[jj] = f2bf(wv[jj]);
       }
     }
     __syncthreads();
     short8 af0 = *(const short8*)&As[(w*16 + m16)*72 + q*8];
     short8 af1 = *(const short8*)&As[(w*16 + m16)*72 + 32 + q*8];
     #pragma unroll
-    for (int j = 0; j < 4; ++j){
+    for (int j = 0; j < 8; ++j){
       short8 b0 = *(const short8*)&Ws[(j*16 + m16)*72 + q*8];
       acc[j] = __builtin_amdgcn_mfma_f32_16x16x32_bf16(af0, b0, acc[j], 0, 0, 0);
-      short8 b1 = *(const short8*)&Ws[(j*16 + m16)*72 + 32 + q*8];
-      acc[j] = __builtin_amdgcn_mfma_f32_16x16x32_bf16(af1, b1, acc[j], 0, 0, 0);
-    }
-    __syncthreads();
-  }
-  #pragma unroll
-  for (int j = 0; j < 4; ++j){
+      short8 b1v = *(const short8*)&Ws[(j*16 + m16)*72 + 32 + q*8];
+      acc[j] = __builtin_amdgcn_mfma_f32_16x16x32_bf16(af1, b1v, acc[j], 0, 0, 0);
+    }
+    __syncthreads();
+  }
+  float val[8][4];
+  #pragma unroll
+  for (int j = 0; j < 8; ++j){
     int n = bn + j*16 + m16;
-    if (n < N){
-      float bv = bias ? bias[n] : 0.f;
-      float gv = 0.f, bbv = 0.f;
-      if (ACT == 1){ gv = gz[n] * BNS; bbv = bbp[n]; }
-      #pragma unroll
-      for (int r = 0; r < 4; ++r){
-        int m = bm + w*16 + q*4 + r;
-        float v = acc[j][r] + bv;
-        if (ACT == 1){ v = v * gv + bbv; v = fmaxf(v, 0.f); }
-        if constexpr (sizeof(CT) == 2) C[(size_t)m*ldc + n] = __float2bfloat16(v);
-        else                           C[(size_t)m*ldc + n] = v;
-      }
-    }
-  }
+    float bv = b2[n];
+    #pragma unroll
+    for (int r = 0; r < 4; ++r) val[j][r] = acc[j][r] + bv;
+  }
+  float* mat = (float*)As;
+  #pragma unroll
+  for (int j = 0; j < 8; ++j){
+    float lm = fmaxf(fmaxf(val[j][0], val[j][1]), fmaxf(val[j][2], val[j][3]));
+    mat[(w*4 + q)*128 + j*16 + m16] = lm;
+  }
+  bf16* C = F3b + 256;
+  #pragma unroll
+  for (int j = 0; j < 8; ++j){
+    int n = bn + j*16 + m16;
+    #pragma unroll
+    for (int r = 0; r < 4; ++r){
+      int m = bm + w*16 + q*4 + r;
+      C[(size_t)m*512 + n] = __float2bfloat16(val[j][r]);
+    }
+  }
+  __syncthreads();
+  int col = t & 127, half = t >> 7;
+  float gm = mat[(half*8)*128 + col];
+  #pragma unroll
+  for (int s = 1; s < 8; ++s) gm = fmaxf(gm, mat[(half*8 + s)*128 + col]);
+  bf16 gb = __float2bfloat16(gm);
+  bf16* dstm = F3b + (size_t)(bm + half*32)*512 + bn + col;
+  #pragma unroll
+  for (int rr = 0; rr < 32; ++rr) dstm[(size_t)rr*512] = gb;
 }
 
 template<typename AT, typename WT, int ACT, typename CT, int POOL>
@@ -332,10 +269,8 @@
   __shared__ __align__(16) short Ws[128*72];
   int bm = blockIdx.x * 64, bn = blockIdx.y * 128;
   int t = threadIdx.x;
-  int row = t >> 2;
-  int kseg = (t & 3) * 16;
-  int row2 = t >> 1;
-  int kseg2 = (t & 1) * 32;
+  int row = t >> 2, kseg = (t & 3) * 16;
+  int row2 = t >> 1, kseg2 = (t & 1) * 32;
   int w = t >> 6, lane = t & 63, m16 = lane & 15, q = lane >> 4;
   floatx4 acc[8] = {};
   for (int k0 = 0; k0 < K; k0 += 64){
@@ -348,9 +283,9 @@
       float a[16];
       #pragma unroll
       for (int j = 0; j < 4; ++j) *(float4*)&a[j*4] = *(const float4*)(Ar + j*4);
-      short* dst = &As[row*72 + kseg];
+      short* dstp = &As[row*72 + kseg];
       #pragma unroll
-      for (int jj = 0; jj < 16; ++jj) dst[jj] = f2bf(a[jj]);
+      for (int jj = 0; jj < 16; ++jj) dstp[jj] = f2bf(a[jj]);
     }
     {
       int n = bn + row2;
@@ -370,17 +305,17 @@
         *(short8*)&Ws[row2*72 + kseg2 + 16] = v2;
         *(short8*)&Ws[row2*72 + kseg2 + 24] = v3;
       } else {
-        short* dst = &Ws[row2*72 + kseg2];
+        short* dstp = &Ws[row2*72 + kseg2];
         if (n < N){
           const float* Wr = (const float*)W + (size_t)n*K + k0 + kseg2;
           float wv[32];
           #pragma unroll
           for (int j = 0; j < 8; ++j) *(float4*)&wv[j*4] = *(const float4*)(Wr + j*4);
           #pragma unroll
-          for (int jj = 0; jj < 32; ++jj) dst[jj] = f2bf(wv[jj]);
+          for (int jj = 0; jj < 32; ++jj) dstp[jj] = f2bf(wv[jj]);
         } else {
           #pragma unroll
-          for (int jj = 0; jj < 32; ++jj) dst[jj] = 0;
+          for (int jj = 0; jj < 32; ++jj) dstp[jj] = 0;
         }
       }
     }
@@ -430,30 +365,109 @@
       float lm = fmaxf(fmaxf(val[j][0], val[j][1]), fmaxf(val[j][2], val[j][3]));
       mat[(w*4 + q)*128 + j*16 + m16] = lm;
     }
-    if constexpr (POOL == 1){
-      #pragma unroll
-      for (int j = 0; j < 8; ++j){
-        int n = bn + j*16 + m16;
-        #pragma unroll
-        for (int r = 0; r < 4; ++r){
-          int m = bm + w*16 + q*4 + r;
-          C[(size_t)m*ldc + n] = __float2bfloat16(val[j][r]);
-        }
-      }
-    }
     __syncthreads();
     int col = t & 127, half = t >> 7;
     float gm = mat[(half*8)*128 + col];
     #pragma unroll
     for (int s = 1; s < 8; ++s) gm = fmaxf(gm, mat[(half*8 + s)*128 + col]);
-    if constexpr (POOL == 1){
-      bf16 gb = __float2bfloat16(gm);
-      bf16* dst = (bf16*)C - 256 + (size_t)(bm + half*32)*ldc + bn + col;
+    int g = (bm >> 5) + half;
+    ((float*)C)[(size_t)g*ldc + bn + col] = gm;
+  }
+}
+
+template<typename AT, typename WT, int ACT, int MODE, typename CT = float>
+__global__ __launch_bounds__(256) void gemm_mfma64(const AT* __restrict__ A, int lda,
+                                                   const WT* __restrict__ W,
+                                                   const float* __restrict__ bias,
+                                                   const float* __restrict__ gz,
+                                                   const float* __restrict__ bbp,
+                                                   CT* __restrict__ C, int ldc,
+                                                   int M, int N, int K){
+  __shared__ __align__(16) short As[64*72];
+  __shared__ __align__(16) short Ws[64*72];
+  int bm = blockIdx.x * 64, bn = blockIdx.y * 64;
+  int t = threadIdx.x;
+  int row = t >> 2, kseg = (t & 3) * 16;
+  int w = t >> 6, lane = t & 63, m16 = lane & 15, q = lane >> 4;
+  floatx4 acc[4] = {};
+  for (int k0 = 0; k0 < K; k0 += 64){
+    if constexpr (MODE == 1){
+      const float* Yr = (const float*)A + (size_t)(bm + row)*lda + k0 + kseg;
+      const float* Zr = gz + (size_t)(bm + row)*1536 + 768 + k0 + kseg;
+      float y[16], z[16];
       #pragma unroll
-      for (int rr = 0; rr < 32; ++rr) dst[(size_t)rr*ldc] = gb;
+      for (int j = 0; j < 4; ++j){
+        *(float4*)&y[j*4] = *(const float4*)(Yr + j*4);
+        *(float4*)&z[j*4] = *(const float4*)(Zr + j*4);
+      }
+      short* dstp = &As[row*72 + kseg];
+      #pragma unroll
+      for (int jj = 0; jj < 16; ++jj) dstp[jj] = f2bf(y[jj] * (z[jj] * fsig(z[jj])));
+    } else if constexpr (sizeof(AT) == 2){
+      const short* Ar = (const short*)A + (size_t)(bm + row)*lda + k0 + kseg;
+      *(short8*)&As[row*72 + kseg]     = *(const short8*)Ar;
+      *(short8*)&As[row*72 + kseg + 8] = *(const short8*)(Ar + 8);
     } else {
-      int g = (bm >> 5) + half;
-      ((float*)C)[(size_t)g*ldc + bn + col] = gm;
+      const float* Ar = (const float*)A + (size_t)(bm + row)*lda + k0 + kseg;
+      float a[16];
+      #pragma unroll
+      for (int j = 0; j < 4; ++j) *(float4*)&a[j*4] = *(const float4*)(Ar + j*4);
+      short* dstp = &As[row*72 + kseg];
+      #pragma unroll
+      for (int jj = 0; jj < 16; ++jj) dstp[jj] = f2bf(a[jj]);
+    }
+    {
+      int n = bn + row;
+      if constexpr (sizeof(WT) == 2){
+        short8 v0, v1;
+        #pragma unroll
+        for (int j = 0; j < 8; ++j){ v0[j] = 0; v1[j] = 0; }
+        if (n < N){
+          const short* Wr = (const short*)W + (size_t)n*K + k0 + kseg;
+          v0 = *(const short8*)Wr;
+          v1 = *(const short8*)(Wr + 8);
+        }
+        *(short8*)&Ws[row*72 + kseg]     = v0;
+        *(short8*)&Ws[row*72 + kseg + 8] = v1;
+      } else {
+        short* dstp = &Ws[row*72 + kseg];
+        if (n < N){
+          const float* Wr = (const float*)W + (size_t)n*K + k0 + kseg;
+          float wv[16];
+          #pragma unroll
+          for (int j = 0; j < 4; ++j) *(float4*)&wv[j*4] = *(const float4*)(Wr + j*4);
+          #pragma unroll
+          for (int jj = 0; jj < 16; ++jj) dstp[jj] = f2bf(wv[jj]);
+        } else {
+          #pragma unroll
+          for (int jj = 0; jj < 16; ++jj) dstp[jj] = 0;
+        }
+      }
+    }
+    __syncthreads();
+    short8 af0 = *(const short8*)&As[(w*16 + m16)*72 + q*8];
+    short8 af1 = *(const short8*)&As[(w*16 + m16)*72 + 32 + q*8];
+    #pragma unroll
+    for (int j = 0; j < 4; ++j){
+      short8 b0 = *(const short8*)&Ws[(j*16 + m16)*72 + q*8];
+      acc[j] = __builtin_amdgcn_mfma_f32_16x16x32_bf16(af0, b0, acc[j], 0, 0, 0);
+      short8 b1 = *(const short8*)&Ws[(j*16 + m16)*72 + 32 + q*8];
+      acc[j] = __builtin_amdgcn_mfma_f32_16x16x32_bf16(af1, b1, acc[j], 0, 0, 0);
+    }
+    __syncthreads();
+  }
+  #pragma unroll
+  for (int j = 0; j < 4; ++j){
+    int n = bn + j*16 + m16;
+    if (n < N){
+      float bv = bias ? bias[n] : 0.f;
+      #pragma unroll
+      for (int r = 0; r < 4; ++r){
+        int m = bm + w*16 + q*4 + r;
+        float v = acc[j][r] + bv;
+        if constexpr (sizeof(CT) == 2) C[(size_t)m*ldc + n] = __float2bfloat16(v);
+        else                           C[(size_t)m*ldc + n] = v;
+      }
     }
   }
 }
@@ -489,13 +503,13 @@
         *(float4*)&x1[j4*4] = (l >= 2) ? *(const float4*)(base - 2*1536 + j4*4) : z4;
         *(float4*)&x0[j4*4] = (l >= 3) ? *(const float4*)(base - 3*1536 + j4*4) : z4;
       }
-      short* dst = &As[row*72 + kseg];
+      short* dstp = &As[row*72 + kseg];
       #pragma unroll
       for (int j = 0; j < 16; ++j){
         float4 wv = *(const float4*)(cw + (size_t)(ch + j)*4);
         float v = x0[j]*wv.x + x1[j]*wv.y + x2[j]*wv.z + x3[j]*wv.w + cb[ch + j];
         v = v * fsig(v);
-        dst[j] = f2bf(v);
+        dstp[j] = f2bf(v);
       }
     }
     {
@@ -512,17 +526,17 @@
         *(short8*)&Ws[row*72 + kseg]     = v0;
         *(short8*)&Ws[row*72 + kseg + 8] = v1;
       } else {
-        short* dst = &Ws[row*72 + kseg];
+        short* dstp = &Ws[row*72 + kseg];
         if (n < 56){
           const float* Wr = (const float*)W + (size_t)n*DI + k0 + kseg;
           float wv[16];
           #pragma unroll
           for (int j = 0; j < 4; ++j) *(float4*)&wv[j*4] = *(const float4*)(Wr + j*4);
           #pragma unroll
-          for (int jj = 0; jj < 16; ++jj) dst[jj] = f2bf(wv[jj]);
+          for (int jj = 0; jj < 16; ++jj) dstp[jj] = f2bf(wv[jj]);
         } else {
           #pragma unroll
-          for (int jj = 0; jj < 16; ++jj) dst[jj] = 0;
+          for (int jj = 0; jj < 16; ++jj) dstp[jj] = 0;
         }
       }
     }
@@ -552,65 +566,68 @@
   }
 }
 
-__global__ __launch_bounds__(256) void maxk_fg(float* __restrict__ f3in){
-  int gg = blockIdx.x; int c = threadIdx.x;
-  float m = -3e38f;
-  for (int k = 0; k < Kn; ++k) m = fmaxf(m, f3in[((size_t)gg*Kn + k)*512 + 256 + c]);
-  for (int k = 0; k < Kn; ++k) f3in[((size_t)gg*Kn + k)*512 + c] = m;
-}
-
-__global__ __launch_bounds__(384) void maxk_tok(const float* __restrict__ f4, float* __restrict__ tok){
-  int gg = blockIdx.x; int c = threadIdx.x;
-  float m = -3e38f;
-  for (int k = 0; k < Kn; ++k) m = fmaxf(m, f4[((size_t)gg*Kn + k)*DM + c]);
-  tok[(size_t)gg*DM + c] = m;
-}
-
-__global__ __launch_bounds__(128) void pos_kernel(const float* __restrict__ center,
-                                                  const float* __restrict__ w1, const float* __restrict__ b1,
-                                                  const float* __restrict__ w2, const float* __restrict__ b2,
-                                                  float* __restrict__ tok){
-  int gid = blockIdx.x;
+__global__ __launch_bounds__(128) void pos_sort_kernel(const float* __restrict__ center,
+    const float* __restrict__ w1, const float* __restrict__ b1,
+    const float* __restrict__ w2, const float* __restrict__ b2,
+    float* __restrict__ tok, int* __restrict__ order){
   __shared__ float h1[128]; __shared__ float c3[3];
-  int t = threadIdx.x;
-  if (t < 3) c3[t] = center[(size_t)gid*3 + t];
-  __syncthreads();
-  float a = w1[t*3+0]*c3[0] + w1[t*3+1]*c3[1] + w1[t*3+2]*c3[2] + b1[t];
-  h1[t] = 0.5f * a * (1.f + erff(a * 0.70710678118654752440f));
-  __syncthreads();
-  for (int c = t; c < DM; c += 128){
-    float s = b2[c];
-    for (int j = 0; j < 128; ++j) s += w2[(size_t)c*128 + j] * h1[j];
-    tok[(size_t)gid*DM + c] += s;
-  }
-}
-
-__global__ __launch_bounds__(128) void sort_kernel(const float* __restrict__ center,
-                                                   int* __restrict__ order){
-  int bax = blockIdx.x; int b = bax / 3, ax = bax % 3;
   __shared__ float key[128];
   int t = threadIdx.x;
-  key[t] = center[(size_t)(b*Gn + t)*3 + ax];
-  __syncthreads();
-  float kt = key[t]; int r = 0;
-  for (int j = 0; j < Gn; ++j){
-    float kj = key[j];
-    r += (kj < kt || (kj == kt && j < t)) ? 1 : 0;
-  }
-  r = min(max(r, 0), Gn-1);
-  order[b*Ln + ax*Gn + r] = t;
-}
-
-__global__ __launch_bounds__(256) void build_h(const float* __restrict__ tok,
-                        const int* __restrict__ order,
-                        float* __restrict__ h, float* __restrict__ res){
-  int i = blockIdx.x * blockDim.x + threadIdx.x;
-  if (i >= Bn*Ln*DM) return;
-  int c = i % DM; int l = (i / DM) % Ln; int b = i / (DM*Ln);
-  int src = order[b*Ln + l];
+  if (blockIdx.x < Bn*Gn){
+    int gid = blockIdx.x;
+    if (t < 3) c3[t] = center[(size_t)gid*3 + t];
+    __syncthreads();
+    float a = w1[t*3+0]*c3[0] + w1[t*3+1]*c3[1] + w1[t*3+2]*c3[2] + b1[t];
+    h1[t] = 0.5f * a * (1.f + erff(a * 0.70710678118654752440f));
+    __syncthreads();
+    for (int c = t; c < DM; c += 128){
+      float s = b2[c];
+      for (int j = 0; j < 128; ++j) s += w2[(size_t)c*128 + j] * h1[j];
+      tok[(size_t)gid*DM + c] += s;
+    }
+  } else {
+    int bax = blockIdx.x - Bn*Gn; int b = bax / 3, ax = bax % 3;
+    key[t] = center[(size_t)(b*Gn + t)*3 + ax];
+    __syncthreads();
+    float kt = key[t]; int r = 0;
+    for (int j = 0; j < Gn; ++j){
+      float kj = key[j];
+      r += (kj < kt || (kj == kt && j < t)) ? 1 : 0;
+    }
+    r = min(max(r, 0), Gn-1);
+    order[b*Ln + ax*Gn + r] = t;
+  }
+}
+
+__global__ __launch_bounds__(256) void ln_res_first(const float* __restrict__ tok,
+                                                    const int* __restrict__ order,
+                                                    float* __restrict__ res,
+                                                    bf16* __restrict__ x,
+                                                    const float* __restrict__ w,
+                                                    const float* __restrict__ bias){
+  int wv = threadIdx.x >> 6, ln = threadIdx.x & 63;
+  int tokid = blockIdx.x*4 + wv;
+  int b = tokid / Ln;
+  int src = order[tokid];
   src = min(max(src, 0), Gn-1);
-  h[i] = tok[((size_t)(b*Gn + src))*DM + c];
-  res[i] = 0.f;
+  const float* hr = tok + ((size_t)(b*Gn + src))*DM;
+  float* rr = res + (size_t)tokid*DM;
+  bf16* xr = x + (size_t)tokid*DM;
+  float v[6]; float s = 0.f;
+  #pragma unroll
+  for (int i = 0; i < 6; ++i){ int c = ln + 64*i; float t = hr[c]; rr[c] = t; v[i] = t; s += t; }
+  #pragma unroll
+  for (int o = 32; o > 0; o >>= 1) s += __shfl_xor(s, o);
+  float mu = s * (1.f/DM);
+  float q = 0.f;
+  #pragma unroll
+  for (int i = 0; i < 6; ++i){ float d = v[i] - mu; q += d*d; }
+  #pragma unroll
+  for (int o = 32; o > 0; o >>= 1) q += __shfl_xor(q, o);
+  float rstd = rsqrtf(q * (1.f/DM) + EPSf);
+  #pragma unroll
+  for (int i = 0; i < 6; ++i){ int c = ln + 64*i;
+    xr[c] = __float2bfloat16((v[i]-mu)*rstd*w[c] + bias[c]); }
 }
 
 __global__ __launch_bounds__(256) void ln_res_kernel(const float* __restrict__ h,
@@ -641,7 +658,7 @@
 }
 
 __global__ __launch_bounds__(256) void scanA_kernel(const float* __restrict__ xz,
-                                                    const float* __restrict__ xdbp, int nks,
+                                                    const float* __restrict__ xdbp,
                                                     const float* __restrict__ cw,
                                                     const float* __restrict__ cb,
                                                     const float* __restrict__ dpw,
@@ -656,12 +673,8 @@
   int c = blk % NCH; int bd = blk / NCH; int dch = bd % 3; int b = bd / 3;
   int t = threadIdx.x; int d = dch*256 + t;
   int l0 = c*CHS;
-  for (int i = t; i < CHS*56; i += 256){
-    size_t base = ((size_t)(b*Ln + l0))*56 + i;
-    float s = xdbp[base];
-    for (int k = 1; k < nks; ++k) s += xdbp[(size_t)k*XDBS + base];
-    sRow[i] = s;
-  }
+  for (int i = t; i < CHS*56; i += 256)
+    sRow[i] = xdbp[((size_t)(b*Ln + l0))*56 + i];
   float xv[CHS+3];
   #pragma unroll
   for (int j = 0; j < 3; ++j){
@@ -710,7 +723,7 @@
 }
 
 __global__ __launch_bounds__(256) void scanB_kernel(float* __restrict__ xz,
-                                                    const float* __restrict__ xdbp, int nks,
+                                                    const float* __restrict__ xdbp,
                                                     const float* __restrict__ cw,
                                                     const float* __restrict__ cb,
                                                     const float* __restrict__ dpw,
@@ -719,20 +732,15 @@
                                                     const float* __restrict__ Dp,
                                                     const float* __restrict__ SB_S,
                                                     const float* __restrict__ SB_dt,
-                                                    const float* __restrict__ BND,
-                                                    bf16* __restrict__ yb){
+                                                    const float* __restrict__ BND){
   __shared__ float sRow[CHS*56];
   __shared__ float sU[CHS*256];
   int blk = blockIdx.x;
   int c = blk % NCH; int bd = blk / NCH; int dch = bd % 3; int b = bd / 3;
   int t = threadIdx.x; int d = dch*256 + t;
   int l0 = c*CHS;
-  for (int i = t; i < CHS*56; i += 256){
-    size_t base = ((size_t)(b*Ln + l0))*56 + i;
-    float s = xdbp[base];
-    for (int k = 1; k < nks; ++k) s += xdbp[(size_t)k*XDBS + base];
-    sRow[i] = s;
-  }
+  for (int i = t; i < CHS*56; i += 256)
+    sRow[i] = xdbp[((size_t)(b*Ln + l0))*56 + i];
   float xv[CHS+3];
   #pragma unroll
   for (int j = 0; j < 3; ++j) xv[j] = BND[((size_t)blk*3 + j)*256 + t];
@@ -764,8 +772,6 @@
   float dbias = dpb[d];
   float Dd = Dp[d];
   float* ydst = xz + ((size_t)(b*Ln + l0))*1536 + dch*256;
-  const float* zrow = xz + ((size_t)(b*Ln + l0))*1536 + 768 + dch*256;
-  bf16* ybr = yb ? (yb + ((size_t)(b*Ln + l0))*DI + dch*256) : nullptr;
   __syncthreads();
   for (int i = 0; i < CHS; ++i){
     int ro = i*56;
@@ -781,13 +787,7 @@
       h[s] = exp2f(dtv * a2[s]) * h[s] + du * sRow[ro + 24 + s];
       yv += h[s] * sRow[ro + 40 + s];
     }
-    float yfull = yv + u*Dd;
-    if (ybr){
-      float zv = zrow[(size_t)i*1536 + t];
-      ybr[(size_t)i*DI + t] = __float2bfloat16(yfull * (zv * fsig(zv)));
-    } else {
-      ydst[(size_t)i*1536 + t] = yfull;
-    }
+    ydst[(size_t)i*1536 + t] = yv + u*Dd;
   }
 }
 
@@ -889,9 +889,7 @@
   constexpr size_t WS_FLOATS = 3919936;
   if (ws_size < WS_FLOATS * sizeof(float)) return;
   constexpr size_t MIDF = 5812224;
-  constexpr size_t BIGF = 9437184;
   const bool mid = ws_size >= (WS_FLOATS + MIDF) * sizeof(float);
-  const bool big = ws_size >= (WS_FLOATS + MIDF + BIGF) * sizeof(float);
 
   const float* pts       = (const float*)d_in[0];
   const float* enc_w1    = (const float*)d_in[1];  const float* enc_b1    = (const float*)d_in[2];
@@ -925,14 +923,14 @@
   float* nb     = U + 1536;
   float* tok    = U + 50688;
   int*   order  = (int*)(U + 247296);
-  float* eb0    = U + 262144;
-  float* eb1    = U + 1310720;
+  bf16*  F3b    = (bf16*)(U + 262144);
+  bf16*  F3c    = (bf16*)(U + 1310720);
   float* xz   = U;
   float* xdb  = U + 2359296;
   bf16*  xb   = (bf16*)(U + 2445312);
-  float* SBdt_s = U + 2445312;
+  float* SBdt = U + 2445312;
   float* BND  = U + 2482176;
-  float* SBS_s  = hb;
+  float* SBS  = hb;
   float* xf   = U;
   float* featp = U + 589824;
   float* WB = ws + WS_FLOATS;
@@ -942,66 +940,33 @@
   bf16* wb_e2 = (bf16*)(WB + 5566464);
   bf16* wb_e3 = (bf16*)(WB + 5582848);
   bf16* wb_e4 = (bf16*)(WB + 5713920);
-  float* BIGB = WB + MIDF;
-  bf16*  F1b  = (bf16*)BIGB;
-  bf16*  F3b  = (bf16*)(BIGB + 1048576);
-  bf16*  F3c  = (bf16*)(BIGB + 5242880);
-  float* xdbp_b = BIGB;
-  float* SBS_b  = BIGB + 344064;
-  float* SBdt_b = BIGB + 933888;
-  bf16*  yb     = (bf16*)(BIGB + 970752);
-
-  if (mid)
-    cvt_all<<<11352, 256, 0, stream>>>(in_proj_w, out_proj_w, x_proj_w,
-                                       enc_w2, enc_w3, enc_w4, (bf16*)WB);
-
-  fps_kernel<<<Bn, 256, 0, stream>>>(pts, center);
+
+  front_kernel<<<mid ? (Bn + 11352) : Bn, 256, 0, stream>>>(pts, center,
+      in_proj_w, out_proj_w, x_proj_w, enc_w2, enc_w3, enc_w4, (bf16*)WB);
   knn_kernel<<<Bn*Gn, 256, 0, stream>>>(pts, center, nb);
 
-  if (big){
-    gemm_mfma<float,float,1,0,bf16><<<dim3(256,2), 256, 0, stream>>>(nb, 3, enc_w1, enc_b1,
-        enc_bn1_g, enc_bn1_b, F1b, 128, 16384, 128, 3);
-    gemm_mfma128<bf16,bf16,0,bf16,1><<<dim3(256,2), 256, 0, stream>>>(F1b, 128, wb_e2, enc_b2,
-        nullptr, nullptr, F3b + 256, 512, 16384, 256, 128);
-    gemm_mfma128<bf16,bf16,1,bf16,0><<<dim3(256,4), 256, 0, stream>>>(F3b, 512, wb_e3, enc_b3,
-        enc_bn2_g, enc_bn2_b, F3c, 512, 16384, 512, 512);
-    gemm_mfma128<bf16,bf16,0,float,2><<<dim3(256,3), 256, 0, stream>>>(F3c, 512, wb_e4, enc_b4,
-        nullptr, nullptr, tok, DM, 16384, 384, 512);
-  } else {
-    for (int ch = 0; ch < 8; ++ch){
-      const float* nb_c = nb + (size_t)ch*2048*3;
-      float* tok_c = tok + (size_t)ch*64*DM;
-      gemm_mfma<float,float,1,0><<<dim3(32,2), 256, 0, stream>>>(nb_c, 3, enc_w1, enc_b1,
-          enc_bn1_g, enc_bn1_b, eb1, 128, 2048, 128, 3);
-      if (mid){
-        gemm_mfma64<float,bf16,0,0><<<dim3(32,4), 256, 0, stream>>>(eb1, 128, wb_e2, enc_b2,
-            nullptr, nullptr, eb0 + 256, 512, 2048, 256, 128);
-        maxk_fg<<<64, 256, 0, stream>>>(eb0);
-        gemm_mfma64<float,bf16,1,0><<<dim3(32,8), 256, 0, stream>>>(eb0, 512, wb_e3, enc_b3,
-            enc_bn2_g, enc_bn2_b, eb1, 512, 2048, 512, 512);
-        gemm_mfma64<float,bf16,0,0><<<dim3(32,6), 256, 0, stream>>>(eb1, 512, wb_e4, enc_b4,
-            nullptr, nullptr, eb0, 384, 2048, 384, 512);
-      } else {
-        gemm_mfma64<float,float,0,0><<<dim3(32,4), 256, 0, stream>>>(eb1, 128, enc_w2, enc_b2,
-            nullptr, nullptr, eb0 + 256, 512, 2048, 256, 128);
-        maxk_fg<<<64, 256, 0, stream>>>(eb0);
-        gemm_mfma64<float,float,1,0><<<dim3(32,8), 256, 0, stream>>>(eb0, 512, enc_w3, enc_b3,
-            enc_bn2_g, enc_bn2_b, eb1, 512, 2048, 512, 512);
-        gemm_mfma64<float,float,0,0><<<dim3(32,6), 256, 0, stream>>>(eb1, 512, enc_w4, enc_b4,
-            nullptr, nullptr, eb0, 384, 2048, 384, 512);
-      }
-      maxk_tok<<<64, 384, 0, stream>>>(eb0, tok_c);
-    }
-  }
-
-  pos_kernel<<<Bn*Gn, 128, 0, stream>>>(center, pos_w1, pos_b1, pos_w2, pos_b2, tok);
-  sort_kernel<<<Bn*3, 128, 0, stream>>>(center, order);
-  build_h<<<(Bn*Ln*DM + 255)/256, 256, 0, stream>>>(tok, order, hb, resb);
-
-  const int nks = big ? 4 : 1;
-  float* xdbp = big ? xdbp_b : xdb;
-  float* SBS  = big ? SBS_b  : SBS_s;
-  float* SBdt = big ? SBdt_b : SBdt_s;
+  for (int b = 0; b < Bn; ++b){
+    const float* nbc = nb + (size_t)b*MC*3;
+    float* tokc = tok + (size_t)b*Gn*DM;
+    if (mid){
+      enc2_kernel<bf16><<<dim3(64,2), 256, 0, stream>>>(nbc, enc_w1, enc_b1,
+          enc_bn1_g, enc_bn1_b, wb_e2, enc_b2, F3b);
+      gemm_mfma128<bf16,bf16,1,bf16,0><<<dim3(64,4), 256, 0, stream>>>(F3b, 512,
+          wb_e3, enc_b3, enc_bn2_g, enc_bn2_b, F3c, 512, MC, 512, 512);
+      gemm_mfma128<bf16,bf16,0,float,2><<<dim3(64,3), 256, 0, stream>>>(F3c, 512,
+          wb_e4, enc_b4, nullptr, nullptr, (float*)tokc, DM, MC, 384, 512);
+    } else {
+      enc2_kernel<float><<<dim3(64,2), 256, 0, stream>>>(nbc, enc_w1, enc_b1,
+          enc_bn1_g, enc_bn1_b, enc_w2, enc_b2, F3b);
+      gemm_mfma128<bf16,float,1,bf16,0><<<dim3(64,4), 256, 0, stream>>>(F3b, 512,
+          enc_w3, enc_b3, enc_bn2_g, enc_bn2_b, F3c, 512, MC, 512, 512);
+      gemm_mfma128<bf16,float,0,float,2><<<dim3(64,3), 256, 0, stream>>>(F3c, 512,
+          enc_w4, enc_b4, nullptr, nullptr, (float*)tokc, DM, MC, 384, 512);
+    }
+  }
+
+  pos_sort_kernel<<<Bn*Gn + Bn*3, 128, 0, stream>>>(center, pos_w1, pos_b1,
+      pos_w2, pos_b2, tok, order);
 
   for (int l = 0; l < DEPTH; ++l){
     const float* lnw  = ln_w      + (size_t)l*DM;
@@ -1016,28 +981,25 @@
     const float* Dpar = D_param   + (size_t)l*DI;
     const float* opw  = out_proj_w+ (size_t)l*DM*DI;
 
-    ln_res_kernel<<<Bn*Ln/4, 256, 0, stream>>>(hb, resb, xb, lnw, lnb);
+    if (l == 0)
+      ln_res_first<<<Bn*Ln/4, 256, 0, stream>>>(tok, order, resb, xb, lnw, lnb);
+    else
+      ln_res_kernel<<<Bn*Ln/4, 256, 0, stream>>>(hb, resb, xb, lnw, lnb);
     if (mid){
       gemm_mfma128<bf16,bf16,0,float,0><<<dim3(24,12), 256, 0, stream>>>(xb, DM,
           wb_ip + (size_t)l*1536*DM, nullptr, nullptr, nullptr, xz, 1536, Bn*Ln, 1536, DM);
+      xproj_kernel<bf16><<<dim3(24,1), 256, 0, stream>>>(xz,
+          wb_xp + (size_t)l*56*DI, cw, cb, xdb, DI);
     } else {
       gemm_mfma128<bf16,float,0,float,0><<<dim3(24,12), 256, 0, stream>>>(xb, DM, ipw,
           nullptr, nullptr, nullptr, xz, 1536, Bn*Ln, 1536, DM);
-    }
-    if (mid)
-      xproj_kernel<bf16><<<dim3(24, nks), 256, 0, stream>>>(xz,
-          wb_xp + (size_t)l*56*DI, cw, cb, xdbp, DI/nks);
-    else
-      xproj_kernel<float><<<dim3(24, nks), 256, 0, stream>>>(xz,
-          xpw, cw, cb, xdbp, DI/nks);
-    scanA_kernel<<<Bn*3*NCH, 256, 0, stream>>>(xz, xdbp, nks, cw, cb,
+      xproj_kernel<float><<<dim3(24,1), 256, 0, stream>>>(xz, xpw, cw, cb, xdb, DI);
+    }
+    scanA_kernel<<<Bn*3*NCH, 256, 0, stream>>>(xz, xdb, cw, cb,
         dpw, dpb, Alg, SBS, SBdt, BND);
-    scanB_kernel<<<Bn*3*NCH, 256, 0, stream>>>(xz, xdbp, nks, cw, cb,
-        dpw, dpb, Alg, Dpar, SBS, SBdt, BND, big ? yb : nullptr);
-    if (big){
-      gemm_mfma64<bf16,bf16,0,0><<<dim3(24,6), 256, 0, stream>>>(yb, DI,
-          wb_op + (size_t)l*DM*DI, nullptr, nullptr, nullptr, hb, DM, Bn*Ln, DM, DI);
-    } else if (mid){
+    scanB_kernel<<<Bn*3*NCH, 256, 0, stream>>>(xz, xdb, cw, cb,
+        dpw, dpb, Alg, Dpar, SBS, SBdt, BND);
+    if (mid){
       gemm_mfma64<float,bf16,0,1><<<dim3(24,6), 256, 0, stream>>>(xz, 1536,
           wb_op + (size_t)l*DM*DI, nullptr, xz, nullptr, hb, DM, Bn*Ln, DM, DI);
     } else {
```

Result: slower. 2.642 ms (+46.7%).
